# Performance work log

Measured on AMD Instinct MI355X. Metric: run time of the kernel, lower is better.

The kernel has to match this reference:

```python
import jax, jax.numpy as jnp
import numpy as np

NQ = 6; DM = 128; CH = 4; SEQ = 2048; CHUNK = 16; BATCH = 128
NFP = 5 * NQ * 2   # feature params for 2 layers
NMP = 5 * NQ * 2   # mixing params for 2 layers

# ---- batched gate matrices (theta: (B,)) ----

def _rx(t):
    c = jnp.cos(t / 2).astype(jnp.complex64)
    s = (-1j * jnp.sin(t / 2)).astype(jnp.complex64)
    return jnp.stack([jnp.stack([c, s], -1), jnp.stack([s, c], -1)], -2)

def _ry(t):
    c = jnp.cos(t / 2).astype(jnp.complex64)
    s = jnp.sin(t / 2).astype(jnp.complex64)
    return jnp.stack([jnp.stack([c, -s], -1), jnp.stack([s, c], -1)], -2)

def _rz(t):
    e = jnp.exp(-1j * t.astype(jnp.complex64) / 2)
    z = jnp.zeros_like(e)
    return jnp.stack([jnp.stack([e, z], -1), jnp.stack([z, jnp.conj(e)], -1)], -2)

def _crx(t):
    B = t.shape[0]
    r = _rx(t)
    I = jnp.broadcast_to(jnp.eye(2, dtype=jnp.complex64), (B, 2, 2))
    Z = jnp.zeros((B, 2, 2), jnp.complex64)
    return jnp.concatenate([jnp.concatenate([I, Z], -1), jnp.concatenate([Z, r], -1)], -2)

# ---- batched statevector gate application; state: (B, 2, ..., 2) with axis 1+w = wire w ----

def _ap1(s, U, w):
    s = jnp.moveaxis(s, 1 + w, 1)
    sh = s.shape
    s = jnp.einsum('bij,bjr->bir', U, s.reshape(sh[0], 2, -1)).reshape(sh)
    return jnp.moveaxis(s, 1, 1 + w)

def _ap2(s, U, w0, w1):
    s = jnp.moveaxis(s, (1 + w0, 1 + w1), (1, 2))
    sh = s.shape
    s = jnp.einsum('bij,bjr->bir', U, s.reshape(sh[0], 4, -1)).reshape(sh)
    return jnp.moveaxis(s, (1, 2), (1 + w0, 1 + w1))

def _ansatz(s, p, off):
    # RX,RY,RZ on each qubit, then forward CRX ring, then backward CRX ring
    for i in range(NQ):
        s = _ap1(s, _rx(p[:, off + 3 * i]), i)
        s = _ap1(s, _ry(p[:, off + 3 * i + 1]), i)
        s = _ap1(s, _rz(p[:, off + 3 * i + 2]), i)
    off += 3 * NQ
    for i in range(NQ):
        s = _ap2(s, _crx(p[:, off]), i, (i + 1) % NQ)
        off += 1
    for i in range(NQ - 1, -1, -1):
        s = _ap2(s, _crx(p[:, off]), i, (i - 1) % NQ)
        off += 1
    return s, off

def _circuit(angles, fp, mp):
    B = angles.shape[0]
    s = jnp.zeros((B, 2 ** NQ), jnp.complex64).at[:, 0].set(1.0).reshape((B,) + (2,) * NQ)
    for i in range(NQ):                      # RY input embedding
        s = _ap1(s, _ry(angles[:, i]), i)
    off = 0
    for _ in range(2):                        # feature layers
        s, off = _ansatz(s, fp, off)
    off = 0
    for _ in range(2):                        # mixing layers
        s, off = _ansatz(s, mp, off)
    xs, ys, zs = [], [], []
    for i in range(NQ):                       # <X_i>, <Y_i>, <Z_i>
        v = jnp.moveaxis(s, 1 + i, 1).reshape(B, 2, -1)
        a, b = v[:, 0], v[:, 1]
        ab = jnp.sum(jnp.conj(a) * b, -1)
        xs.append(2 * jnp.real(ab))
        ys.append(2 * jnp.imag(ab))
        zs.append(jnp.sum(jnp.abs(a) ** 2 - jnp.abs(b) ** 2, -1))
    return jnp.stack(xs + ys + zs, 1)         # (B, 18) ordered X..Y..Z

def _ln(x, g, b, eps=1e-5):
    m = x.mean(-1, keepdims=True)
    v = ((x - m) ** 2).mean(-1, keepdims=True)
    return (x - m) / jnp.sqrt(v + eps) * g + b

def _fwd(x, conv_w, conv_b, ln1_g, ln1_b, ca1_w, ca1_b, ca2_w, ca2_b, pp_w, pp_b,
         ep_w, ep_b, op_w, op_b, ln2_g, ln2_b, sa1_w, sa1_b, sa2_w, sa2_b,
         cl1_w, cl1_b, cl2_w, cl2_b):
    B, C, S = x.shape
    h = jax.lax.conv_general_dilated(x, conv_w, (1,), [(1, 1)],
                                     dimension_numbers=('NCH', 'OIH', 'NCH')) + conv_b[None, :, None]
    h = jnp.transpose(h, (0, 2, 1))           # (B, S, D)
    h = _ln(h, ln1_g, ln1_b)
    nchunks = S // CHUNK
    h = h.reshape(B * nchunks, CHUNK, DM)
    sc = jnp.tanh(h @ ca1_w + ca1_b) @ ca2_w + ca2_b
    w = jax.nn.softmax(sc, axis=1)
    summ = jnp.sum(w * h, axis=1)             # (B*nchunks, D)
    ap = summ @ pp_w + pp_b
    fp, mp = ap[:, :NFP], ap[:, NFP:]
    ang = jnp.tanh(summ @ ep_w + ep_b) * np.pi
    q = _circuit(ang, fp, mp)                 # (B*nchunks, 18)
    cf = jax.nn.silu(_ln(q @ op_w + op_b, ln2_g, ln2_b))  # dropout = eval identity
    cf = cf.reshape(B, nchunks, DM)
    ss = jnp.tanh(cf @ sa1_w + sa1_b) @ sa2_w + sa2_b
    sw = jax.nn.softmax(ss, axis=1)
    rep = jnp.sum(sw * cf, axis=1)
    return jax.nn.silu(rep @ cl1_w + cl1_b) @ cl2_w + cl2_b

def setup_inputs() -> dict:
    key = jax.random.key(0)
    ks = jax.random.split(key, 16)
    n = lambda k, sh: (jax.random.normal(k, sh, jnp.float32) * 0.05)
    return {
        'x': jax.random.normal(ks[0], (BATCH, CH, SEQ), jnp.float32),
        'conv_w': n(ks[1], (DM, CH, 3)), 'conv_b': jnp.zeros((DM,), jnp.float32),
        'ln1_g': jnp.ones((DM,), jnp.float32), 'ln1_b': jnp.zeros((DM,), jnp.float32),
        'ca1_w': n(ks[2], (DM, DM // 4)), 'ca1_b': jnp.zeros((DM // 4,), jnp.float32),
        'ca2_w': n(ks[3], (DM // 4, 1)), 'ca2_b': jnp.zeros((1,), jnp.float32),
        'pp_w': n(ks[4], (DM, NFP + NMP)), 'pp_b': jnp.zeros((NFP + NMP,), jnp.float32),
        'ep_w': n(ks[5], (DM, NQ)), 'ep_b': jnp.zeros((NQ,), jnp.float32),
        'op_w': n(ks[6], (3 * NQ, DM)), 'op_b': jnp.zeros((DM,), jnp.float32),
        'ln2_g': jnp.ones((DM,), jnp.float32), 'ln2_b': jnp.zeros((DM,), jnp.float32),
        'sa1_w': n(ks[7], (DM, DM // 4)), 'sa1_b': jnp.zeros((DM // 4,), jnp.float32),
        'sa2_w': n(ks[8], (DM // 4, 1)), 'sa2_b': jnp.zeros((1,), jnp.float32),
        'cl1_w': n(ks[9], (DM, DM // 2)), 'cl1_b': jnp.zeros((DM // 2,), jnp.float32),
        'cl2_w': n(ks[10], (DM // 2, 2)), 'cl2_b': jnp.zeros((2,), jnp.float32),
    }

def reference(x, conv_w, conv_b, ln1_g, ln1_b, ca1_w, ca1_b, ca2_w, ca2_b, pp_w, pp_b,
              ep_w, ep_b, op_w, op_b, ln2_g, ln2_b, sa1_w, sa1_b, sa2_w, sa2_b,
              cl1_w, cl1_b, cl2_w, cl2_b):
    return _fwd(x, conv_w, conv_b, ln1_g, ln1_b, ca1_w, ca1_b, ca2_w, ca2_b, pp_w, pp_b,
                ep_w, ep_b, op_w, op_b, ln2_g, ln2_b, sa1_w, sa1_b, sa2_w, sa2_b,
                cl1_w, cl1_b, cl2_w, cl2_b)
```

## Files before the change

### kernel.cpp

```cpp
#include <hip/hip_runtime.h>
#include <math.h>


constexpr int kNQ    = 6;
constexpr int kDM    = 128;
constexpr int kCH    = 4;
constexpr int kSEQ   = 2048;
constexpr int kCHUNK = 16;
constexpr int kBATCH = 128;
constexpr int kNCH   = kSEQ / kCHUNK;
constexpr int kNP    = 120;
constexpr float kPI  = 3.14159265358979323846f;

typedef __attribute__((ext_vector_type(8))) short bf16x8;
typedef __attribute__((ext_vector_type(4))) float f32x4;

__device__ __forceinline__ float fast_tanh(float x) {
  float e = __expf(-2.f * fabsf(x));
  float r = (1.f - e) * __builtin_amdgcn_rcpf(1.f + e);
  return copysignf(r, x);
}
__device__ __forceinline__ float fast_silu(float x) {
  return x * __builtin_amdgcn_rcpf(1.f + __expf(-x));
}

template <int XM>
__device__ __forceinline__ float qp(float v) {
  constexpr int ctrl = (XM == 1) ? 0xB1 : 0x4E;
  return __int_as_float(
      __builtin_amdgcn_update_dpp(0, __float_as_int(v), ctrl, 0xF, 0xF, true));
}


template <int RB>
__device__ __forceinline__ void rx_reg(float c, float s, float* sr, float* si) {
#pragma unroll
  for (int r0 = 0; r0 < 16; ++r0) {
    if (r0 & RB) continue;
    int r1 = r0 | RB;
    float ar = sr[r0], ai = si[r0], br = sr[r1], bi = si[r1];
    sr[r0] = fmaf(c, ar,  s * bi);  si[r0] = fmaf(c, ai, -s * br);
    sr[r1] = fmaf(c, br,  s * ai);  si[r1] = fmaf(c, bi, -s * ar);
  }
}

template <int RB>
__device__ __forceinline__ void ry_reg(float c, float s, float* sr, float* si) {
#pragma unroll
  for (int r0 = 0; r0 < 16; ++r0) {
    if (r0 & RB) continue;
    int r1 = r0 | RB;
    float ar = sr[r0], ai = si[r0], br = sr[r1], bi = si[r1];
    sr[r0] = fmaf(c, ar, -s * br);  si[r0] = fmaf(c, ai, -s * bi);
    sr[r1] = fmaf(s, ar,  c * br);  si[r1] = fmaf(s, ai,  c * bi);
  }
}

template <int RB>
__device__ __forceinline__ void rz_reg(float c, float s, float* sr, float* si) {
#pragma unroll
  for (int r = 0; r < 16; ++r) {
    float sp = (r & RB) ? s : -s;
    float ar = sr[r], ai = si[r];
    sr[r] = fmaf(c, ar, -sp * ai);
    si[r] = fmaf(c, ai,  sp * ar);
  }
}

template <int XM>
__device__ __forceinline__ void rx_lane(float c, float s, float* sr, float* si) {
#pragma unroll
  for (int r = 0; r < 16; ++r) {
    float pr = qp<XM>(sr[r]), pi = qp<XM>(si[r]);
    sr[r] = fmaf(c, sr[r],  s * pi);
    si[r] = fmaf(c, si[r], -s * pr);
  }
}

template <int XM>
__device__ __forceinline__ void ry_lane(float c, float sg, float* sr, float* si) {
#pragma unroll
  for (int r = 0; r < 16; ++r) {
    float pr = qp<XM>(sr[r]), pi = qp<XM>(si[r]);
    sr[r] = fmaf(c, sr[r], sg * pr);
    si[r] = fmaf(c, si[r], sg * pi);
  }
}

__device__ __forceinline__ void rz_lane(float c, float sp, float* sr, float* si) {
#pragma unroll
  for (int r = 0; r < 16; ++r) {
    float ar = sr[r], ai = si[r];
    sr[r] = fmaf(c, ar, -sp * ai);
    si[r] = fmaf(c, ai,  sp * ar);
  }
}

template <int RB, int CB>
__device__ __forceinline__ void crx_reg_reg(float c, float s, float* sr, float* si) {
#pragma unroll
  for (int r0 = 0; r0 < 16; ++r0) {
    if ((r0 & RB) || !(r0 & CB)) continue;
    int r1 = r0 | RB;
    float ar = sr[r0], ai = si[r0], br = sr[r1], bi = si[r1];
    sr[r0] = fmaf(c, ar,  s * bi);  si[r0] = fmaf(c, ai, -s * br);
    sr[r1] = fmaf(c, br,  s * ai);  si[r1] = fmaf(c, bi, -s * ar);
  }
}

template <int XM, int CB>
__device__ __forceinline__ void crx_reg_lane(float c, float s, float* sr, float* si) {
#pragma unroll
  for (int r = 0; r < 16; ++r) {
    if (!(r & CB)) continue;
    float pr = qp<XM>(sr[r]), pi = qp<XM>(si[r]);
    sr[r] = fmaf(c, sr[r],  s * pi);
    si[r] = fmaf(c, si[r], -s * pr);
  }
}

template <int RB>
__device__ __forceinline__ void meas_reg(const float* sr, const float* si,
                                         float& tr, float& ti, float& zz) {
  tr = 0.f; ti = 0.f; zz = 0.f;
#pragma unroll
  for (int r0 = 0; r0 < 16; ++r0) {
    float n = fmaf(sr[r0], sr[r0], si[r0] * si[r0]);
    zz += (r0 & RB) ? -n : n;
    if (r0 & RB) continue;
    int r1 = r0 | RB;
    tr = fmaf(sr[r0], sr[r1], fmaf(si[r0], si[r1], tr));
    ti = fmaf(sr[r0], si[r1], fmaf(-si[r0], sr[r1], ti));
  }
  tr += qp<1>(tr); tr += qp<2>(tr);
  ti += qp<1>(ti); ti += qp<2>(ti);
  zz += qp<1>(zz); zz += qp<2>(zz);
}


__global__ __launch_bounds__(128) void k_pre8(
    const float* __restrict__ x,
    const float* __restrict__ conv_w, const float* __restrict__ conv_b,
    const float* __restrict__ ln1_g,  const float* __restrict__ ln1_b,
    const float* __restrict__ ca1_w,  const float* __restrict__ ca1_b,
    const float* __restrict__ ca2_w,  const float* __restrict__ ca2_b,
    const float* __restrict__ pp_w,   const float* __restrict__ pp_b,
    const float* __restrict__ ep_w,   const float* __restrict__ ep_b,
    float* __restrict__ outb, int emit_cs)
{
  constexpr int NC = 8;

  __shared__ __align__(16) float xs[kCH][NC * kCHUNK + 4];
  __shared__ __align__(16) float hbuf[kCHUNK][132];
  __shared__ __align__(16) float spart[2][16];
  __shared__ __align__(16) float wl[kCHUNK];
  __shared__ __align__(16) float sums[NC][kDM];
  __shared__ float mrow[kCHUNK], irow[kCHUNK];

  const int tid    = threadIdx.x;
  const int chunk0 = blockIdx.x * NC;
  const int b      = chunk0 >> 7;
  const int tloc   = (chunk0 & 127) * kCHUNK;
  const int d      = tid;
  const int lane   = tid & 63;
  const int wv     = tid >> 6;
  const int col    = (lane & 15) + 16 * wv;
  const int qd     = lane >> 4;

  float w12[12];
  {
    const float4* cw = (const float4*)(conv_w + d * 12);
    float4 a0 = cw[0], a1 = cw[1], a2 = cw[2];
    w12[0]=a0.x; w12[1]=a0.y; w12[2]=a0.z; w12[3]=a0.w;
    w12[4]=a1.x; w12[5]=a1.y; w12[6]=a1.z; w12[7]=a1.w;
    w12[8]=a2.x; w12[9]=a2.y; w12[10]=a2.z; w12[11]=a2.w;
  }
  float cb = conv_b[d];
  float g1 = ln1_g[d], b1 = ln1_b[d];
  float cb1 = ca1_b[col], cw2 = ca2_w[col], cb2 = ca2_b[0];

  bf16x8 bhi[4], blo[4];
#pragma unroll
  for (int ks = 0; ks < 4; ++ks)
#pragma unroll
    for (int jj = 0; jj < 8; ++jj) {
      float bvf = ca1_w[(ks * 32 + qd * 8 + jj) * 32 + col];
      unsigned bb = __float_as_uint(bvf);
      bhi[ks][jj] = (short)(bb >> 16);
      float lf = bvf - __uint_as_float(bb & 0xffff0000u);
      blo[ks][jj] = (short)(__float_as_uint(lf) >> 16);
    }

#pragma unroll
  for (int ch = 0; ch < kCH; ++ch) {
#pragma unroll
    for (int base = 0; base < 2; ++base) {
      int pos = base * 128 + tid;
      if (pos < NC * kCHUNK + 2) {
        int s = tloc - 1 + pos;
        float v = 0.f;
        if (s >= 0 && s < kSEQ) v = x[((size_t)b * kCH + ch) * kSEQ + s];
        xs[ch][pos] = v;
      }
    }
  }
  __syncthreads();

  for (int c = 0; c < NC; ++c) {
    float h[kCHUNK];
#pragma unroll
    for (int t = 0; t < kCHUNK; ++t) h[t] = cb;
#pragma unroll
    for (int ch = 0; ch < kCH; ++ch) {
      const float4* xp = (const float4*)&xs[ch][c * kCHUNK];
      float4 v0 = xp[0], v1 = xp[1], v2 = xp[2], v3 = xp[3], v4 = xp[4];
      float xr[18];
      xr[0]=v0.x; xr[1]=v0.y; xr[2]=v0.z; xr[3]=v0.w;
      xr[4]=v1.x; xr[5]=v1.y; xr[6]=v1.z; xr[7]=v1.w;
      xr[8]=v2.x; xr[9]=v2.y; xr[10]=v2.z; xr[11]=v2.w;
      xr[12]=v3.x; xr[13]=v3.y; xr[14]=v3.z; xr[15]=v3.w;
      xr[16]=v4.x; xr[17]=v4.y;
      float c0 = w12[ch*3+0], c1 = w12[ch*3+1], c2 = w12[ch*3+2];
#pragma unroll
      for (int t = 0; t < kCHUNK; ++t)
        h[t] = fmaf(xr[t], c0, fmaf(xr[t+1], c1, fmaf(xr[t+2], c2, h[t])));
    }
#pragma unroll
    for (int t = 0; t < kCHUNK; ++t) hbuf[t][d] = h[t];
    __syncthreads();

    {
      int row = tid >> 3, k = tid & 7;
      const float4* rp = (const float4*)&hbuf[row][k * 16];
      float s1 = 0.f, s2 = 0.f;
#pragma unroll
      for (int q = 0; q < 4; ++q) {
        float4 v = rp[q];
        s1 += v.x + v.y + v.z + v.w;
        s2 = fmaf(v.x,v.x,s2); s2 = fmaf(v.y,v.y,s2);
        s2 = fmaf(v.z,v.z,s2); s2 = fmaf(v.w,v.w,s2);
      }
#pragma unroll
      for (int o = 1; o < 8; o <<= 1) {
        s1 += __shfl_xor(s1, o, 64);
        s2 += __shfl_xor(s2, o, 64);
      }
      if (k == 0) {
        float m = s1 * (1.f / kDM);
        mrow[row] = m;
        irow[row] = rsqrtf(s2 * (1.f / kDM) - m * m + 1e-5f);
      }
    }
    __syncthreads();

#pragma unroll
    for (int t = 0; t < kCHUNK; ++t) {
      h[t] = fmaf((h[t] - mrow[t]) * irow[t], g1, b1);
      unsigned hb = __float_as_uint(h[t]);
      float lof = h[t] - __uint_as_float(hb & 0xffff0000u);
      unsigned pk = (hb >> 16) | (__float_as_uint(lof) & 0xffff0000u);
      ((unsigned*)&hbuf[t][0])[d] = pk;
    }
    __syncthreads();

    f32x4 acc = {0.f, 0.f, 0.f, 0.f};
    {
      const unsigned* hrow = (const unsigned*)&hbuf[lane & 15][0];
#pragma unroll
      for (int ks = 0; ks < 4; ++ks) {
        const uint4* ap = (const uint4*)(hrow + ks * 32 + qd * 8);
        uint4 w0 = ap[0], w1 = ap[1];
        bf16x8 ahi, alo;
        ahi[0] = (short)(w0.x & 0xffff); ahi[1] = (short)(w0.y & 0xffff);
        ahi[2] = (short)(w0.z & 0xffff); ahi[3] = (short)(w0.w & 0xffff);
        ahi[4] = (short)(w1.x & 0xffff); ahi[5] = (short)(w1.y & 0xffff);
        ahi[6] = (short)(w1.z & 0xffff); ahi[7] = (short)(w1.w & 0xffff);
        alo[0] = (short)(w0.x >> 16); alo[1] = (short)(w0.y >> 16);
        alo[2] = (short)(w0.z >> 16); alo[3] = (short)(w0.w >> 16);
        alo[4] = (short)(w1.x >> 16); alo[5] = (short)(w1.y >> 16);
        alo[6] = (short)(w1.z >> 16); alo[7] = (short)(w1.w >> 16);
        acc = __builtin_amdgcn_mfma_f32_16x16x32_bf16(ahi, bhi[ks], acc, 0, 0, 0);
        acc = __builtin_amdgcn_mfma_f32_16x16x32_bf16(ahi, blo[ks], acc, 0, 0, 0);
        acc = __builtin_amdgcn_mfma_f32_16x16x32_bf16(alo, bhi[ks], acc, 0, 0, 0);
      }
    }

    {
      float ev[4];
#pragma unroll
      for (int r = 0; r < 4; ++r)
        ev[r] = fast_tanh(acc[r] + cb1) * cw2;
#pragma unroll
      for (int o = 1; o < 16; o <<= 1)
#pragma unroll
        for (int r = 0; r < 4; ++r) ev[r] += __shfl_xor(ev[r], o, 64);
      if ((lane & 15) == 0)
        *(float4*)&spart[wv][qd * 4] = make_float4(ev[0], ev[1], ev[2], ev[3]);
    }
    __syncthreads();

    if (tid < 16) {
      float scl = spart[0][tid] + spart[1][tid] + cb2;
      float mx = scl;
#pragma unroll
      for (int o = 1; o < 16; o <<= 1) mx = fmaxf(mx, __shfl_xor(mx, o, 64));
      float e = __expf(scl - mx);
      float se = e;
#pragma unroll
      for (int o = 1; o < 16; o <<= 1) se += __shfl_xor(se, o, 64);
      wl[tid] = e * (1.f / se);
    }
    __syncthreads();

    {
      const float4* w4 = (const float4*)wl;
      float4 wa = w4[0], wb = w4[1], wc = w4[2], wd = w4[3];
      float acc2 = 0.f;
      acc2 = fmaf(wa.x, h[0],  acc2); acc2 = fmaf(wa.y, h[1],  acc2);
      acc2 = fmaf(wa.z, h[2],  acc2); acc2 = fmaf(wa.w, h[3],  acc2);
      acc2 = fmaf(wb.x, h[4],  acc2); acc2 = fmaf(wb.y, h[5],  acc2);
      acc2 = fmaf(wb.z, h[6],  acc2); acc2 = fmaf(wb.w, h[7],  acc2);
      acc2 = fmaf(wc.x, h[8],  acc2); acc2 = fmaf(wc.y, h[9],  acc2);
      acc2 = fmaf(wc.z, h[10], acc2); acc2 = fmaf(wc.w, h[11], acc2);
      acc2 = fmaf(wd.x, h[12], acc2); acc2 = fmaf(wd.y, h[13], acc2);
      acc2 = fmaf(wd.z, h[14], acc2); acc2 = fmaf(wd.w, h[15], acc2);
      sums[c][d] = acc2;
    }
  }
  __syncthreads();

  if (tid < kNP + kNQ) {
    const bool isep = (tid >= kNP);
    const int  jj   = tid - kNP;
    const float* wp = isep ? (ep_w + jj) : (pp_w + tid);
    const int  ws   = isep ? kNQ : kNP;
    const int  ws2  = ws * 2, ws3 = ws * 3, ws4 = ws * 4;
    float bias = isep ? ep_b[jj] : pp_b[tid];
    float accp[NC];
#pragma unroll
    for (int c = 0; c < NC; ++c) accp[c] = bias;
#pragma unroll 4
    for (int q4 = 0; q4 < 32; ++q4) {
      float w0 = wp[0], w1 = wp[ws], w2 = wp[ws2], w3 = wp[ws3];
      wp += ws4;
#pragma unroll
      for (int c = 0; c < NC; ++c) {
        float4 s = *(const float4*)&sums[c][q4 * 4];
        accp[c] = fmaf(s.x, w0, fmaf(s.y, w1, fmaf(s.z, w2, fmaf(s.w, w3, accp[c]))));
      }
    }
    const int slot = isep ? jj : (6 + tid);
#pragma unroll
    for (int c = 0; c < NC; ++c) {
      int chunkg = chunk0 + c;
      float ha = isep ? (0.5f * fast_tanh(accp[c]) * kPI) : (0.5f * accp[c]);
      if (emit_cs) {
        ((float2*)(outb + (size_t)chunkg * 256))[slot] =
            make_float2(__cosf(ha), __sinf(ha));
      } else {
        outb[(size_t)chunkg * 126 + slot] = ha;
      }
    }
  }
}


constexpr int kCsStride = 260;

__global__ __launch_bounds__(64) void k_circ_cs(const float* __restrict__ csA,
                                                float* __restrict__ qv_g)
{
  __shared__ __align__(16) float lds[16 * kCsStride];

  const int lane  = threadIdx.x;
  const int c     = lane >> 2;
  const int l     = lane & 3;
  const int chunk = blockIdx.x * 16 + c;
  const int b0 = (l >> 1) & 1;
  const int b1 = l & 1;

  {
    const float4* src = (const float4*)(csA + (size_t)blockIdx.x * 16 * 256);
#pragma unroll
    for (int i = 0; i < 16; ++i) {
      float4 v = src[i * 64 + lane];
      *(float4*)&lds[i * kCsStride + lane * 4] = v;
    }
  }
  __syncthreads();

  const float2* cp = (const float2*)&lds[c * kCsStride];

  float sr[16], si[16];
#pragma unroll
  for (int r = 0; r < 16; ++r) { sr[r] = 0.f; si[r] = 0.f; }
  sr[0] = (l == 0) ? 1.f : 0.f;

  {
    float2 q0 = cp[0], q1 = cp[1], q2 = cp[2], q3 = cp[3], q4 = cp[4], q5 = cp[5];
    ry_lane<2>(q0.x, b0 ? q0.y : -q0.y, sr, si);
    ry_lane<1>(q1.x, b1 ? q1.y : -q1.y, sr, si);
    ry_reg<8>(q2.x, q2.y, sr, si);
    ry_reg<4>(q3.x, q3.y, sr, si);
    ry_reg<2>(q4.x, q4.y, sr, si);
    ry_reg<1>(q5.x, q5.y, sr, si);
  }

  for (int a = 0; a < 4; ++a) {
    const float2* pb = cp + 6 + a * 30;
    float2 t;
    t = pb[0];  rx_lane<2>(t.x, t.y, sr, si);
    t = pb[1];  ry_lane<2>(t.x, b0 ? t.y : -t.y, sr, si);
    t = pb[2];  rz_lane   (t.x, b0 ? t.y : -t.y, sr, si);
    t = pb[3];  rx_lane<1>(t.x, t.y, sr, si);
    t = pb[4];  ry_lane<1>(t.x, b1 ? t.y : -t.y, sr, si);
    t = pb[5];  rz_lane   (t.x, b1 ? t.y : -t.y, sr, si);
    t = pb[6];  rx_reg<8>(t.x, t.y, sr, si);
    t = pb[7];  ry_reg<8>(t.x, t.y, sr, si);
    t = pb[8];  rz_reg<8>(t.x, t.y, sr, si);
    t = pb[9];  rx_reg<4>(t.x, t.y, sr, si);
    t = pb[10]; ry_reg<4>(t.x, t.y, sr, si);
    t = pb[11]; rz_reg<4>(t.x, t.y, sr, si);
    t = pb[12]; rx_reg<2>(t.x, t.y, sr, si);
    t = pb[13]; ry_reg<2>(t.x, t.y, sr, si);
    t = pb[14]; rz_reg<2>(t.x, t.y, sr, si);
    t = pb[15]; rx_reg<1>(t.x, t.y, sr, si);
    t = pb[16]; ry_reg<1>(t.x, t.y, sr, si);
    t = pb[17]; rz_reg<1>(t.x, t.y, sr, si);
    t = pb[18]; { float c2 = b0 ? t.x : 1.f, s2 = b0 ? t.y : 0.f; rx_lane<1>(c2, s2, sr, si); }
    t = pb[19]; { float c2 = b1 ? t.x : 1.f, s2 = b1 ? t.y : 0.f; rx_reg<8>(c2, s2, sr, si); }
    t = pb[20]; crx_reg_reg<4, 8>(t.x, t.y, sr, si);
    t = pb[21]; crx_reg_reg<2, 4>(t.x, t.y, sr, si);
    t = pb[22]; crx_reg_reg<1, 2>(t.x, t.y, sr, si);
    t = pb[23]; crx_reg_lane<2, 1>(t.x, t.y, sr, si);
    t = pb[24]; crx_reg_reg<2, 1>(t.x, t.y, sr, si);
    t = pb[25]; crx_reg_reg<4, 2>(t.x, t.y, sr, si);
    t = pb[26]; crx_reg_reg<8, 4>(t.x, t.y, sr, si);
    t = pb[27]; crx_reg_lane<1, 8>(t.x, t.y, sr, si);
    t = pb[28]; { float c2 = b1 ? t.x : 1.f, s2 = b1 ? t.y : 0.f; rx_lane<2>(c2, s2, sr, si); }
    t = pb[29]; { float c2 = b0 ? t.x : 1.f, s2 = b0 ? t.y : 0.f; rx_reg<1>(c2, s2, sr, si); }
  }

  float res[18];
  {
    float tr = 0.f, ti = 0.f, zz = 0.f;
#pragma unroll
    for (int r = 0; r < 16; ++r) {
      float pr = qp<2>(sr[r]), pi = qp<2>(si[r]);
      tr = fmaf(sr[r], pr, fmaf(si[r], pi, tr));
      ti = fmaf(sr[r], pi, fmaf(-si[r], pr, ti));
      zz = fmaf(sr[r], sr[r], fmaf(si[r], si[r], zz));
    }
    tr = b0 ? 0.f : tr;  ti = b0 ? 0.f : ti;  zz = b0 ? -zz : zz;
    tr += qp<1>(tr); tr += qp<2>(tr);
    ti += qp<1>(ti); ti += qp<2>(ti);
    zz += qp<1>(zz); zz += qp<2>(zz);
    res[0] = 2.f * tr; res[6] = 2.f * ti; res[12] = zz;
  }
  {
    float tr = 0.f, ti = 0.f, zz = 0.f;
#pragma unroll
    for (int r = 0; r < 16; ++r) {
      float pr = qp<1>(sr[r]), pi = qp<1>(si[r]);
      tr = fmaf(sr[r], pr, fmaf(si[r], pi, tr));
      ti = fmaf(sr[r], pi, fmaf(-si[r], pr, ti));
      zz = fmaf(sr[r], sr[r], fmaf(si[r], si[r], zz));
    }
    tr = b1 ? 0.f : tr;  ti = b1 ? 0.f : ti;  zz = b1 ? -zz : zz;
    tr += qp<1>(tr); tr += qp<2>(tr);
    ti += qp<1>(ti); ti += qp<2>(ti);
    zz += qp<1>(zz); zz += qp<2>(zz);
    res[1] = 2.f * tr; res[7] = 2.f * ti; res[13] = zz;
  }
  {
    float tr, ti, zz;
    meas_reg<8>(sr, si, tr, ti, zz); res[2] = 2.f*tr; res[8]  = 2.f*ti; res[14] = zz;
    meas_reg<4>(sr, si, tr, ti, zz); res[3] = 2.f*tr; res[9]  = 2.f*ti; res[15] = zz;
    meas_reg<2>(sr, si, tr, ti, zz); res[4] = 2.f*tr; res[10] = 2.f*ti; res[16] = zz;
    meas_reg<1>(sr, si, tr, ti, zz); res[5] = 2.f*tr; res[11] = 2.f*ti; res[17] = zz;
  }
  if (l == 0) {
    float* qo = qv_g + (size_t)chunk * 18;
#pragma unroll
    for (int k = 0; k < 18; ++k) qo[k] = res[k];
  }
}


__global__ __launch_bounds__(64) void k_circ(const float* __restrict__ csb_g,
                                             float* __restrict__ qv_g)
{
  const int lane  = threadIdx.x;
  const int c     = lane >> 2;
  const int l     = lane & 3;
  const int chunk = blockIdx.x * 16 + c;
  const float* cp = csb_g + (size_t)chunk * 126;
  const int b0 = (l >> 1) & 1;
  const int b1 = l & 1;

  float sr[16], si[16];
#pragma unroll
  for (int r = 0; r < 16; ++r) { sr[r] = 0.f; si[r] = 0.f; }
  sr[0] = (l == 0) ? 1.f : 0.f;

  {
    float gc[6], gs[6];
#pragma unroll
    for (int g = 0; g < 6; ++g) { float th = cp[g]; gc[g] = __cosf(th); gs[g] = __sinf(th); }
    ry_lane<2>(gc[0], b0 ? gs[0] : -gs[0], sr, si);
    ry_lane<1>(gc[1], b1 ? gs[1] : -gs[1], sr, si);
    ry_reg<8>(gc[2], gs[2], sr, si);
    ry_reg<4>(gc[3], gs[3], sr, si);
    ry_reg<2>(gc[4], gs[4], sr, si);
    ry_reg<1>(gc[5], gs[5], sr, si);
  }

  for (int a = 0; a < 4; ++a) {
    const float* pb = cp + 6 + a * 30;
    float gc[30], gs[30];
#pragma unroll
    for (int g = 0; g < 30; ++g) { float th = pb[g]; gc[g] = __cosf(th); gs[g] = __sinf(th); }
    rx_lane<2>(gc[0], gs[0], sr, si);
    ry_lane<2>(gc[1], b0 ? gs[1] : -gs[1], sr, si);
    rz_lane   (gc[2], b0 ? gs[2] : -gs[2], sr, si);
    rx_lane<1>(gc[3], gs[3], sr, si);
    ry_lane<1>(gc[4], b1 ? gs[4] : -gs[4], sr, si);
    rz_lane   (gc[5], b1 ? gs[5] : -gs[5], sr, si);
    rx_reg<8>(gc[6],  gs[6],  sr, si);  ry_reg<8>(gc[7],  gs[7],  sr, si);  rz_reg<8>(gc[8],  gs[8],  sr, si);
    rx_reg<4>(gc[9],  gs[9],  sr, si);  ry_reg<4>(gc[10], gs[10], sr, si);  rz_reg<4>(gc[11], gs[11], sr, si);
    rx_reg<2>(gc[12], gs[12], sr, si);  ry_reg<2>(gc[13], gs[13], sr, si);  rz_reg<2>(gc[14], gs[14], sr, si);
    rx_reg<1>(gc[15], gs[15], sr, si);  ry_reg<1>(gc[16], gs[16], sr, si);  rz_reg<1>(gc[17], gs[17], sr, si);
    { float c2 = b0 ? gc[18] : 1.f, s2 = b0 ? gs[18] : 0.f; rx_lane<1>(c2, s2, sr, si); }
    { float c2 = b1 ? gc[19] : 1.f, s2 = b1 ? gs[19] : 0.f; rx_reg<8>(c2, s2, sr, si); }
    crx_reg_reg<4, 8>(gc[20], gs[20], sr, si);
    crx_reg_reg<2, 4>(gc[21], gs[21], sr, si);
    crx_reg_reg<1, 2>(gc[22], gs[22], sr, si);
    crx_reg_lane<2, 1>(gc[23], gs[23], sr, si);
    crx_reg_reg<2, 1>(gc[24], gs[24], sr, si);
    crx_reg_reg<4, 2>(gc[25], gs[25], sr, si);
    crx_reg_reg<8, 4>(gc[26], gs[26], sr, si);
    crx_reg_lane<1, 8>(gc[27], gs[27], sr, si);
    { float c2 = b1 ? gc[28] : 1.f, s2 = b1 ? gs[28] : 0.f; rx_lane<2>(c2, s2, sr, si); }
    { float c2 = b0 ? gc[29] : 1.f, s2 = b0 ? gs[29] : 0.f; rx_reg<1>(c2, s2, sr, si); }
  }

  float res[18];
  {
    float tr = 0.f, ti = 0.f, zz = 0.f;
#pragma unroll
    for (int r = 0; r < 16; ++r) {
      float pr = qp<2>(sr[r]), pi = qp<2>(si[r]);
      tr = fmaf(sr[r], pr, fmaf(si[r], pi, tr));
      ti = fmaf(sr[r], pi, fmaf(-si[r], pr, ti));
      zz = fmaf(sr[r], sr[r], fmaf(si[r], si[r], zz));
    }
    tr = b0 ? 0.f : tr;  ti = b0 ? 0.f : ti;  zz = b0 ? -zz : zz;
    tr += qp<1>(tr); tr += qp<2>(tr);
    ti += qp<1>(ti); ti += qp<2>(ti);
    zz += qp<1>(zz); zz += qp<2>(zz);
    res[0] = 2.f * tr; res[6] = 2.f * ti; res[12] = zz;
  }
  {
    float tr = 0.f, ti = 0.f, zz = 0.f;
#pragma unroll
    for (int r = 0; r < 16; ++r) {
      float pr = qp<1>(sr[r]), pi = qp<1>(si[r]);
      tr = fmaf(sr[r], pr, fmaf(si[r], pi, tr));
      ti = fmaf(sr[r], pi, fmaf(-si[r], pr, ti));
      zz = fmaf(sr[r], sr[r], fmaf(si[r], si[r], zz));
    }
    tr = b1 ? 0.f : tr;  ti = b1 ? 0.f : ti;  zz = b1 ? -zz : zz;
    tr += qp<1>(tr); tr += qp<2>(tr);
    ti += qp<1>(ti); ti += qp<2>(ti);
    zz += qp<1>(zz); zz += qp<2>(zz);
    res[1] = 2.f * tr; res[7] = 2.f * ti; res[13] = zz;
  }
  {
    float tr, ti, zz;
    meas_reg<8>(sr, si, tr, ti, zz); res[2] = 2.f*tr; res[8]  = 2.f*ti; res[14] = zz;
    meas_reg<4>(sr, si, tr, ti, zz); res[3] = 2.f*tr; res[9]  = 2.f*ti; res[15] = zz;
    meas_reg<2>(sr, si, tr, ti, zz); res[4] = 2.f*tr; res[10] = 2.f*ti; res[16] = zz;
    meas_reg<1>(sr, si, tr, ti, zz); res[5] = 2.f*tr; res[11] = 2.f*ti; res[17] = zz;
  }
  if (l == 0) {
    float* qo = qv_g + (size_t)chunk * 18;
#pragma unroll
    for (int k = 0; k < 18; ++k) qo[k] = res[k];
  }
}


__global__ __launch_bounds__(128) void k_post(
    const float* __restrict__ qv_g,
    const float* __restrict__ op_w, const float* __restrict__ op_b,
    const float* __restrict__ ln2_g, const float* __restrict__ ln2_b,
    const float* __restrict__ sa1_w, const float* __restrict__ sa1_b,
    const float* __restrict__ sa2_w, const float* __restrict__ sa2_b,
    float* __restrict__ cf, float* __restrict__ sclb)
{
  __shared__ float cfs[132];
  __shared__ float part1[32];
  __shared__ float red[4];

  const int chunk = blockIdx.x, tid = threadIdx.x, d = tid;
  const int j = tid & 31, sub = tid >> 5;

  float qv[18];
  {
    const float* qpp = qv_g + (size_t)chunk * 18;
#pragma unroll
    for (int k = 0; k < 18; ++k) qv[k] = qpp[k];
  }
  float acc = op_b[d];
#pragma unroll
  for (int k = 0; k < 18; ++k) acc = fmaf(qv[k], op_w[k * kDM + d], acc);

  float v = acc, v2 = acc * acc;
#pragma unroll
  for (int o = 32; o; o >>= 1) { v += __shfl_xor(v, o, 64); v2 += __shfl_xor(v2, o, 64); }
  if ((tid & 63) == 0) { red[tid >> 6] = v; red[2 + (tid >> 6)] = v2; }
  __syncthreads();
  float s1 = red[0] + red[1], s2 = red[2] + red[3];
  float m = s1 * (1.f / kDM);
  float var = s2 * (1.f / kDM) - m * m;
  float xn = fmaf((acc - m) * rsqrtf(var + 1e-5f), ln2_g[d], ln2_b[d]);
  float cfv = fast_silu(xn);
  cf[(size_t)chunk * kDM + d] = cfv;
  cfs[d] = cfv;
  __syncthreads();

  float acc2 = 0.f;
  {
    const float* wp2 = sa1_w + (sub * 32) * 32 + j;
#pragma unroll
    for (int q = 0; q < 8; ++q) {
      float4 hv = *(const float4*)&cfs[sub * 32 + q * 4];
      acc2 = fmaf(hv.x, wp2[(q*4+0)*32], acc2);
      acc2 = fmaf(hv.y, wp2[(q*4+1)*32], acc2);
      acc2 = fmaf(hv.z, wp2[(q*4+2)*32], acc2);
      acc2 = fmaf(hv.w, wp2[(q*4+3)*32], acc2);
    }
  }
  acc2 += __shfl_xor(acc2, 32, 64);
  if (sub == 2) part1[j] = acc2;
  __syncthreads();
  if (tid < 32) {
    float hv = fast_tanh(acc2 + part1[j] + sa1_b[j]) * sa2_w[j];
#pragma unroll
    for (int o = 16; o; o >>= 1) hv += __shfl_xor(hv, o, 64);
    if (j == 0) sclb[chunk] = hv + sa2_b[0];
  }
}


__global__ __launch_bounds__(512) void k_pool_cf(
    const float* __restrict__ cf, const float* __restrict__ scl,
    const float* __restrict__ cl1_w, const float* __restrict__ cl1_b,
    const float* __restrict__ cl2_w, const float* __restrict__ cl2_b,
    float* __restrict__ out)
{
  __shared__ float wl[kNCH];
  __shared__ float rep4[4][kDM];
  __shared__ float ulp[8][64];
  __shared__ float ul[64];
  __shared__ float red2[16];
  int b = blockIdx.x, tid = threadIdx.x;
  int idx = tid & 127, wid = tid >> 6;
  float s = scl[b*kNCH + idx];
  float mx = s;
#pragma unroll
  for (int o = 32; o; o >>= 1) mx = fmaxf(mx, __shfl_xor(mx,o,64));
  if ((tid & 63) == 0) red2[wid] = mx;
  __syncthreads();
  mx = fmaxf(red2[0], red2[1]);
  float e = __expf(s - mx);
  float se = e;
#pragma unroll
  for (int o = 32; o; o >>= 1) se += __shfl_xor(se,o,64);
  if ((tid & 63) == 0) red2[8+wid] = se;
  if (tid < kNCH) wl[tid] = e;
  __syncthreads();
  float inv = 1.f/(red2[8]+red2[9]);
  {
    int dd = tid & 127, qq = tid >> 7;
    const float* cfb = cf + (size_t)b*kNCH*kDM + (size_t)qq*32*kDM;
    const float* wlq = wl + qq*32;
    float a0=0,a1=0,a2=0,a3=0;
#pragma unroll 4
    for (int ncc = 0; ncc < 32; ncc += 4) {
      a0 = fmaf(wlq[ncc+0], cfb[(ncc+0)*kDM+dd], a0);
      a1 = fmaf(wlq[ncc+1], cfb[(ncc+1)*kDM+dd], a1);
      a2 = fmaf(wlq[ncc+2], cfb[(ncc+2)*kDM+dd], a2);
      a3 = fmaf(wlq[ncc+3], cfb[(ncc+3)*kDM+dd], a3);
    }
    rep4[qq][dd] = (a0+a1)+(a2+a3);
  }
  __syncthreads();
  {
    int jj = tid & 63, qq = tid >> 6;
    float accp = 0.f;
#pragma unroll
    for (int k = 0; k < 16; ++k) {
      int dd = qq*16 + k;
      float rv = ((rep4[0][dd]+rep4[1][dd])+(rep4[2][dd]+rep4[3][dd]))*inv;
      accp = fmaf(rv, cl1_w[dd*64+jj], accp);
    }
    ulp[qq][jj] = accp;
  }
  __syncthreads();
  if (tid < 64) {
    float acc = cl1_b[tid];
#pragma unroll
    for (int q = 0; q < 8; ++q) acc += ulp[q][tid];
    ul[tid] = fast_silu(acc);
  }
  __syncthreads();
  if (tid < 2) {
    float acc = cl2_b[tid];
#pragma unroll
    for (int k = 0; k < 64; ++k) acc = fmaf(ul[k], cl2_w[k*2+tid], acc);
    out[b*2+tid] = acc;
  }
}


__device__ __forceinline__ void fb_rx(float2 cs, int w, int lane, float& ar, float& ai) {
  int m = 1 << (5 - w);
  float pr = __shfl_xor(ar, m, 64), pi = __shfl_xor(ai, m, 64);
  float nr = fmaf(cs.x, ar, cs.y * pi), ni = fmaf(cs.x, ai, -cs.y * pr);
  ar = nr; ai = ni;
}
__device__ __forceinline__ void fb_ry(float2 cs, int w, int lane, float& ar, float& ai) {
  int m = 1 << (5 - w);
  float pr = __shfl_xor(ar, m, 64), pi = __shfl_xor(ai, m, 64);
  float sg = ((lane >> (5 - w)) & 1) ? cs.y : -cs.y;
  float nr = fmaf(cs.x, ar, sg * pr), ni = fmaf(cs.x, ai, sg * pi);
  ar = nr; ai = ni;
}
__device__ __forceinline__ void fb_rz(float2 cs, int w, int lane, float& ar, float& ai) {
  float sp = ((lane >> (5 - w)) & 1) ? cs.y : -cs.y;
  float nr = fmaf(ar, cs.x, -ai * sp), ni = fmaf(ar, sp, ai * cs.x);
  ar = nr; ai = ni;
}
__device__ __forceinline__ void fb_crx(float2 cs, int w0, int w1, int lane, float& ar, float& ai) {
  int m = 1 << (5 - w1);
  float pr = __shfl_xor(ar, m, 64), pi = __shfl_xor(ai, m, 64);
  if ((lane >> (5 - w0)) & 1) {
    float nr = fmaf(cs.x, ar, cs.y * pi), ni = fmaf(cs.x, ai, -cs.y * pr);
    ar = nr; ai = ni;
  }
}
__device__ __forceinline__ void fb_ansatz(const float2* cs, int lane, float& ar, float& ai) {
#pragma unroll
  for (int i = 0; i < kNQ; ++i) {
    fb_rx(cs[3*i+0], i, lane, ar, ai);
    fb_ry(cs[3*i+1], i, lane, ar, ai);
    fb_rz(cs[3*i+2], i, lane, ar, ai);
  }
  int off = 18;
#pragma unroll
  for (int i = 0; i < kNQ; ++i) fb_crx(cs[off++], i, (i+1)%kNQ, lane, ar, ai);
#pragma unroll
  for (int i = kNQ-1; i >= 0; --i) fb_crx(cs[off++], i, (i+5)%kNQ, lane, ar, ai);
}

__global__ __launch_bounds__(128) void k_chunk_fb(
    const float* __restrict__ x,
    const float* __restrict__ conv_w, const float* __restrict__ conv_b,
    const float* __restrict__ ln1_g,  const float* __restrict__ ln1_b,
    const float* __restrict__ ca1_w,  const float* __restrict__ ca1_b,
    const float* __restrict__ ca2_w,  const float* __restrict__ ca2_b,
    const float* __restrict__ pp_w,   const float* __restrict__ pp_b,
    const float* __restrict__ ep_w,   const float* __restrict__ ep_b,
    const float* __restrict__ op_w,   const float* __restrict__ op_b,
    const float* __restrict__ ln2_g,  const float* __restrict__ ln2_b,
    float* __restrict__ cf)
{
  __shared__ float hbuf[kCHUNK][132];
  __shared__ __align__(16) float Bu[512];
  __shared__ float mrow[kCHUNK], irow[kCHUNK];
  __shared__ float red[4];
  float (*xs)[kCHUNK+2] = (float(*)[kCHUNK+2])Bu;
  float (*part)[32] = (float(*)[32])Bu;
  float* summ = Bu; float* wl = Bu + 128; float* qv = Bu + 144;
  float2* csb = (float2*)(Bu + 164);

  const int tid = threadIdx.x, chunk = blockIdx.x;
  const int b = chunk >> 7, nc = chunk & 127, t0 = nc * kCHUNK, d = tid;
  const int j = tid & 31, sub = tid >> 5;

  float w12[12];
  {
    const float4* cw = (const float4*)(conv_w + d*12);
    float4 a0=cw[0],a1=cw[1],a2=cw[2];
    w12[0]=a0.x;w12[1]=a0.y;w12[2]=a0.z;w12[3]=a0.w;
    w12[4]=a1.x;w12[5]=a1.y;w12[6]=a1.z;w12[7]=a1.w;
    w12[8]=a2.x;w12[9]=a2.y;w12[10]=a2.z;w12[11]=a2.w;
  }
  float cb = conv_b[d], g1 = ln1_g[d], b1 = ln1_b[d];
  float wreg[32];
  { const float* wp = ca1_w + (sub*32)*32 + j;
#pragma unroll
    for (int k = 0; k < 32; ++k) wreg[k] = wp[k*32]; }

  if (tid < kCH*(kCHUNK+2)) {
    int ch = tid/(kCHUNK+2), pos = tid%(kCHUNK+2), s = t0-1+pos;
    float v = 0.f; if (s >= 0 && s < kSEQ) v = x[(b*kCH+ch)*kSEQ + s];
    xs[ch][pos] = v;
  }
  __syncthreads();
#pragma unroll
  for (int t = 0; t < kCHUNK; ++t) {
    float acc = cb;
#pragma unroll
    for (int ch = 0; ch < kCH; ++ch)
#pragma unroll
      for (int k = 0; k < 3; ++k) acc = fmaf(xs[ch][t+k], w12[ch*3+k], acc);
    hbuf[t][d] = acc;
  }
  __syncthreads();
  {
    int row = tid >> 3, k = tid & 7;
    const float4* rp = (const float4*)&hbuf[row][k*16];
    float s1 = 0.f, s2 = 0.f;
#pragma unroll
    for (int q = 0; q < 4; ++q) {
      float4 v = rp[q];
      s1 += v.x+v.y+v.z+v.w;
      s2 = fmaf(v.x,v.x,s2); s2 = fmaf(v.y,v.y,s2);
      s2 = fmaf(v.z,v.z,s2); s2 = fmaf(v.w,v.w,s2);
    }
#pragma unroll
    for (int o = 1; o < 8; o <<= 1) { s1 += __shfl_xor(s1,o,64); s2 += __shfl_xor(s2,o,64); }
    if (k == 0) {
      float m = s1*(1.f/kDM);
      mrow[row] = m; irow[row] = rsqrtf(s2*(1.f/kDM) - m*m + 1e-5f);
    }
  }
  __syncthreads();
#pragma unroll
  for (int t = 0; t < kCHUNK; ++t)
    hbuf[t][d] = fmaf((hbuf[t][d]-mrow[t])*irow[t], g1, b1);
  __syncthreads();
  float p[kCHUNK];
#pragma unroll
  for (int t = 0; t < kCHUNK; ++t) {
    float acc = 0.f;
#pragma unroll
    for (int qq = 0; qq < 8; ++qq) {
      int q = (qq + 2*sub) & 7;
      float4 v = *(const float4*)&hbuf[t][sub*32 + q*4];
      acc = fmaf(v.x,wreg[q*4+0],acc); acc = fmaf(v.y,wreg[q*4+1],acc);
      acc = fmaf(v.z,wreg[q*4+2],acc); acc = fmaf(v.w,wreg[q*4+3],acc);
    }
    p[t] = acc;
  }
#pragma unroll
  for (int t = 0; t < kCHUNK; ++t) p[t] += __shfl_xor(p[t], 32, 64);
  if (sub == 2) {
#pragma unroll
    for (int t = 0; t < kCHUNK; ++t) part[t][j] = p[t];
  }
  __syncthreads();
  if (tid < 64) {
    float bj = ca1_b[j], w2 = ca2_w[j];
#pragma unroll
    for (int t = 0; t < kCHUNK; ++t) p[t] = fast_tanh(p[t] + part[t][j] + bj) * w2;
#pragma unroll
    for (int o = 16; o; o >>= 1)
#pragma unroll
      for (int t = 0; t < kCHUNK; ++t) p[t] += __shfl_xor(p[t], o, 64);
    float mx = p[0];
#pragma unroll
    for (int t = 1; t < kCHUNK; ++t) mx = fmaxf(mx, p[t]);
    float e[kCHUNK], ssum = 0.f;
#pragma unroll
    for (int t = 0; t < kCHUNK; ++t) { e[t] = __expf(p[t]-mx); ssum += e[t]; }
    float inv = 1.f/ssum;
    if (tid == 0) {
      float4* w4 = (float4*)wl;
      w4[0]=make_float4(e[0]*inv,e[1]*inv,e[2]*inv,e[3]*inv);
      w4[1]=make_float4(e[4]*inv,e[5]*inv,e[6]*inv,e[7]*inv);
      w4[2]=make_float4(e[8]*inv,e[9]*inv,e[10]*inv,e[11]*inv);
      w4[3]=make_float4(e[12]*inv,e[13]*inv,e[14]*inv,e[15]*inv);
    }
  }
  __syncthreads();
  {
    float acc = 0.f;
    const float4* w4 = (const float4*)wl;
#pragma unroll
    for (int tq = 0; tq < 4; ++tq) {
      float4 wv = w4[tq];
      acc = fmaf(wv.x,hbuf[tq*4+0][d],acc); acc = fmaf(wv.y,hbuf[tq*4+1][d],acc);
      acc = fmaf(wv.z,hbuf[tq*4+2][d],acc); acc = fmaf(wv.w,hbuf[tq*4+3][d],acc);
    }
    summ[d] = acc;
  }
  __syncthreads();
  if (tid < kNP) {
    float acc = pp_b[tid];
    const float4* s4 = (const float4*)summ;
#pragma unroll 8
    for (int q = 0; q < 32; ++q) {
      float4 v = s4[q];
      acc = fmaf(v.x,pp_w[(q*4+0)*kNP+tid],acc); acc = fmaf(v.y,pp_w[(q*4+1)*kNP+tid],acc);
      acc = fmaf(v.z,pp_w[(q*4+2)*kNP+tid],acc); acc = fmaf(v.w,pp_w[(q*4+3)*kNP+tid],acc);
    }
    csb[6+tid] = make_float2(__cosf(0.5f*acc), __sinf(0.5f*acc));
  } else if (tid < kNP + kNQ) {
    int jj = tid - kNP;
    float acc = ep_b[jj];
    for (int dd = 0; dd < kDM; ++dd) acc = fmaf(summ[dd], ep_w[dd*kNQ+jj], acc);
    float a = fast_tanh(acc) * kPI;
    csb[jj] = make_float2(__cosf(0.5f*a), __sinf(0.5f*a));
  }
  float ow[18];
#pragma unroll
  for (int jj = 0; jj < 18; ++jj) ow[jj] = op_w[jj*kDM + d];
  float g2 = ln2_g[d], b2 = ln2_b[d], ob = op_b[d];
  __syncthreads();
  if (tid < 64) {
    int lane = tid;
    float ar = (lane == 0) ? 1.f : 0.f, ai = 0.f;
#pragma unroll
    for (int i = 0; i < kNQ; ++i) fb_ry(csb[i], i, lane, ar, ai);
    fb_ansatz(csb+6, lane, ar, ai);  fb_ansatz(csb+36, lane, ar, ai);
    fb_ansatz(csb+66, lane, ar, ai); fb_ansatz(csb+96, lane, ar, ai);
#pragma unroll
    for (int i = 0; i < kNQ; ++i) {
      int m = 1 << (5-i);
      float pr = __shfl_xor(ar, m, 64), pi = __shfl_xor(ai, m, 64);
      int bit = (lane >> (5-i)) & 1;
      float nrm = fmaf(ar,ar,ai*ai);
      float abr, abi, zz;
      if (bit) { abr = 0.f; abi = 0.f; zz = -nrm; }
      else { abr = fmaf(ar,pr,ai*pi); abi = fmaf(ar,pi,-ai*pr); zz = nrm; }
#pragma unroll
      for (int o = 32; o; o >>= 1) {
        abr += __shfl_xor(abr,o,64); abi += __shfl_xor(abi,o,64); zz += __shfl_xor(zz,o,64);
      }
      if (lane == 0) { qv[i] = 2.f*abr; qv[kNQ+i] = 2.f*abi; qv[2*kNQ+i] = zz; }
    }
  }
  __syncthreads();
  {
    float acc = ob;
#pragma unroll
    for (int jj = 0; jj < 18; ++jj) acc = fmaf(qv[jj], ow[jj], acc);
    float v = acc, v2 = acc*acc;
#pragma unroll
    for (int o = 32; o; o >>= 1) { v += __shfl_xor(v,o,64); v2 += __shfl_xor(v2,o,64); }
    if ((tid & 63) == 0) { red[tid>>6] = v; red[2+(tid>>6)] = v2; }
    __syncthreads();
    float s1 = red[0]+red[1], s2 = red[2]+red[3];
    float m = s1*(1.f/kDM), var = s2*(1.f/kDM) - m*m;
    float xn = fmaf((acc-m)*rsqrtf(var+1e-5f), g2, b2);
    cf[(size_t)chunk*kDM + d] = fast_silu(xn);
  }
}

__global__ __launch_bounds__(256) void k_scl_fb(
    const float* __restrict__ cf,
    const float* __restrict__ sa1_w, const float* __restrict__ sa1_b,
    const float* __restrict__ sa2_w, const float* __restrict__ sa2_b,
    float* __restrict__ scl)
{
  int tid = threadIdx.x, wid = tid >> 6, lane = tid & 63;
  int pair = blockIdx.x * 4 + wid;
  int j = lane & 31, hh = lane >> 5;
  const float4* row = (const float4*)(cf + (size_t)pair*kDM + hh*64);
  const float* wp = sa1_w + (hh*64)*32 + j;
  float acc = 0.f;
#pragma unroll
  for (int q = 0; q < 16; ++q) {
    float4 v = row[q];
    acc = fmaf(v.x,wp[(q*4+0)*32],acc); acc = fmaf(v.y,wp[(q*4+1)*32],acc);
    acc = fmaf(v.z,wp[(q*4+2)*32],acc); acc = fmaf(v.w,wp[(q*4+3)*32],acc);
  }
  acc += __shfl_xor(acc, 32, 64);
  float hv = fast_tanh(acc + sa1_b[j]);
  float v = hv * sa2_w[j];
#pragma unroll
  for (int o = 16; o; o >>= 1) v += __shfl_xor(v, o, 64);
  if (lane == 0) scl[pair] = v + sa2_b[0];
}


extern "C" void kernel_launch(void* const* d_in, const int* in_sizes, int n_in,
                              void* d_out, int out_size, void* d_ws, size_t ws_size,
                              hipStream_t stream) {
  const float* x      = (const float*)d_in[0];
  const float* conv_w = (const float*)d_in[1];
  const float* conv_b = (const float*)d_in[2];
  const float* ln1_g  = (const float*)d_in[3];
  const float* ln1_b  = (const float*)d_in[4];
  const float* ca1_w  = (const float*)d_in[5];
  const float* ca1_b  = (const float*)d_in[6];
  const float* ca2_w  = (const float*)d_in[7];
  const float* ca2_b  = (const float*)d_in[8];
  const float* pp_w   = (const float*)d_in[9];
  const float* pp_b   = (const float*)d_in[10];
  const float* ep_w   = (const float*)d_in[11];
  const float* ep_b   = (const float*)d_in[12];
  const float* op_w   = (const float*)d_in[13];
  const float* op_b   = (const float*)d_in[14];
  const float* ln2_g  = (const float*)d_in[15];
  const float* ln2_b  = (const float*)d_in[16];
  const float* sa1_w  = (const float*)d_in[17];
  const float* sa1_b  = (const float*)d_in[18];
  const float* sa2_w  = (const float*)d_in[19];
  const float* sa2_b  = (const float*)d_in[20];
  const float* cl1_w  = (const float*)d_in[21];
  const float* cl1_b  = (const float*)d_in[22];
  const float* cl2_w  = (const float*)d_in[23];
  const float* cl2_b  = (const float*)d_in[24];
  float* out = (float*)d_out;

  const size_t nch   = (size_t)kBATCH * kNCH;
  const size_t fCS   = nch * 256;
  const size_t need1 = (fCS + nch * 18 + nch) * sizeof(float);
  const size_t fA    = nch * kDM;
  const size_t need2 = (fA + nch * 18 + nch) * sizeof(float);

  if (ws_size >= need1) {
    float* csA   = (float*)d_ws;
    float* cf    = csA;
    float* qv_g  = csA + fCS;
    float* sclb  = qv_g + nch * 18;
    k_pre8<<<(kBATCH * kNCH) / 8, 128, 0, stream>>>(
        x, conv_w, conv_b, ln1_g, ln1_b, ca1_w, ca1_b, ca2_w, ca2_b,
        pp_w, pp_b, ep_w, ep_b, csA, 1);
    k_circ_cs<<<(kBATCH * kNCH) / 16, 64, 0, stream>>>(csA, qv_g);
    k_post<<<kBATCH * kNCH, 128, 0, stream>>>(
        qv_g, op_w, op_b, ln2_g, ln2_b, sa1_w, sa1_b, sa2_w, sa2_b, cf, sclb);
    k_pool_cf<<<kBATCH, 512, 0, stream>>>(
        cf, sclb, cl1_w, cl1_b, cl2_w, cl2_b, out);
  } else if (ws_size >= need2) {
    float* A     = (float*)d_ws;
    float* qv_g  = A + fA;
    float* sclb  = qv_g + nch * 18;
    k_pre8<<<(kBATCH * kNCH) / 8, 128, 0, stream>>>(
        x, conv_w, conv_b, ln1_g, ln1_b, ca1_w, ca1_b, ca2_w, ca2_b,
        pp_w, pp_b, ep_w, ep_b, A, 0);
    k_circ<<<(kBATCH * kNCH) / 16, 64, 0, stream>>>(A, qv_g);
    k_post<<<kBATCH * kNCH, 128, 0, stream>>>(
        qv_g, op_w, op_b, ln2_g, ln2_b, sa1_w, sa1_b, sa2_w, sa2_b, A, sclb);
    k_pool_cf<<<kBATCH, 512, 0, stream>>>(
        A, sclb, cl1_w, cl1_b, cl2_w, cl2_b, out);
  } else {
    float* cf   = (float*)d_ws;
    float* sclb = cf + nch * kDM;
    k_chunk_fb<<<kBATCH * kNCH, 128, 0, stream>>>(
        x, conv_w, conv_b, ln1_g, ln1_b, ca1_w, ca1_b, ca2_w, ca2_b,
        pp_w, pp_b, ep_w, ep_b, op_w, op_b, ln2_g, ln2_b, cf);
    k_scl_fb<<<(kBATCH * kNCH) / 4, 256, 0, stream>>>(cf, sa1_w, sa1_b, sa2_w, sa2_b, sclb);
    k_pool_cf<<<kBATCH, 512, 0, stream>>>(cf, sclb, cl1_w, cl1_b, cl2_w, cl2_b, out);
  }
}
```

Measured before the change: 208.2 us.

## Fuse pre, circuit and post kernels into one megakernel per 16 chunks

Merges the conv/LN/attention-pool/param-projection kernel, the statevector circuit simulation and the post-projection/score kernel into a single kernel handling 16 chunks per block. Circuit inputs (cos/sin) and measured expectations stay in shared memory instead of round-tripping through global workspace, and three launches become one. The circuit phase now runs only on 64 of 128 threads, and the post phase loops serially over 16 chunks with barriers. That cuts parallelism and grid size (1024 blocks) and may lower occupancy because of the larger LDS footprint.

Result: slower. 213.8 us (+2.7%).

```diff
diff --git a/kernel.cpp b/kernel.cpp
--- a/kernel.cpp
+++ b/kernel.cpp
@@ -138,259 +138,9 @@
 }
 
 
-__global__ __launch_bounds__(128) void k_pre8(
-    const float* __restrict__ x,
-    const float* __restrict__ conv_w, const float* __restrict__ conv_b,
-    const float* __restrict__ ln1_g,  const float* __restrict__ ln1_b,
-    const float* __restrict__ ca1_w,  const float* __restrict__ ca1_b,
-    const float* __restrict__ ca2_w,  const float* __restrict__ ca2_b,
-    const float* __restrict__ pp_w,   const float* __restrict__ pp_b,
-    const float* __restrict__ ep_w,   const float* __restrict__ ep_b,
-    float* __restrict__ outb, int emit_cs)
-{
-  constexpr int NC = 8;
-
-  __shared__ __align__(16) float xs[kCH][NC * kCHUNK + 4];
-  __shared__ __align__(16) float hbuf[kCHUNK][132];
-  __shared__ __align__(16) float spart[2][16];
-  __shared__ __align__(16) float wl[kCHUNK];
-  __shared__ __align__(16) float sums[NC][kDM];
-  __shared__ float mrow[kCHUNK], irow[kCHUNK];
-
-  const int tid    = threadIdx.x;
-  const int chunk0 = blockIdx.x * NC;
-  const int b      = chunk0 >> 7;
-  const int tloc   = (chunk0 & 127) * kCHUNK;
-  const int d      = tid;
-  const int lane   = tid & 63;
-  const int wv     = tid >> 6;
-  const int col    = (lane & 15) + 16 * wv;
-  const int qd     = lane >> 4;
-
-  float w12[12];
-  {
-    const float4* cw = (const float4*)(conv_w + d * 12);
-    float4 a0 = cw[0], a1 = cw[1], a2 = cw[2];
-    w12[0]=a0.x; w12[1]=a0.y; w12[2]=a0.z; w12[3]=a0.w;
-    w12[4]=a1.x; w12[5]=a1.y; w12[6]=a1.z; w12[7]=a1.w;
-    w12[8]=a2.x; w12[9]=a2.y; w12[10]=a2.z; w12[11]=a2.w;
-  }
-  float cb = conv_b[d];
-  float g1 = ln1_g[d], b1 = ln1_b[d];
-  float cb1 = ca1_b[col], cw2 = ca2_w[col], cb2 = ca2_b[0];
-
-  bf16x8 bhi[4], blo[4];
-#pragma unroll
-  for (int ks = 0; ks < 4; ++ks)
-#pragma unroll
-    for (int jj = 0; jj < 8; ++jj) {
-      float bvf = ca1_w[(ks * 32 + qd * 8 + jj) * 32 + col];
-      unsigned bb = __float_as_uint(bvf);
-      bhi[ks][jj] = (short)(bb >> 16);
-      float lf = bvf - __uint_as_float(bb & 0xffff0000u);
-      blo[ks][jj] = (short)(__float_as_uint(lf) >> 16);
-    }
-
-#pragma unroll
-  for (int ch = 0; ch < kCH; ++ch) {
-#pragma unroll
-    for (int base = 0; base < 2; ++base) {
-      int pos = base * 128 + tid;
-      if (pos < NC * kCHUNK + 2) {
-        int s = tloc - 1 + pos;
-        float v = 0.f;
-        if (s >= 0 && s < kSEQ) v = x[((size_t)b * kCH + ch) * kSEQ + s];
-        xs[ch][pos] = v;
-      }
-    }
-  }
-  __syncthreads();
-
-  for (int c = 0; c < NC; ++c) {
-    float h[kCHUNK];
-#pragma unroll
-    for (int t = 0; t < kCHUNK; ++t) h[t] = cb;
-#pragma unroll
-    for (int ch = 0; ch < kCH; ++ch) {
-      const float4* xp = (const float4*)&xs[ch][c * kCHUNK];
-      float4 v0 = xp[0], v1 = xp[1], v2 = xp[2], v3 = xp[3], v4 = xp[4];
-      float xr[18];
-      xr[0]=v0.x; xr[1]=v0.y; xr[2]=v0.z; xr[3]=v0.w;
-      xr[4]=v1.x; xr[5]=v1.y; xr[6]=v1.z; xr[7]=v1.w;
-      xr[8]=v2.x; xr[9]=v2.y; xr[10]=v2.z; xr[11]=v2.w;
-      xr[12]=v3.x; xr[13]=v3.y; xr[14]=v3.z; xr[15]=v3.w;
-      xr[16]=v4.x; xr[17]=v4.y;
-      float c0 = w12[ch*3+0], c1 = w12[ch*3+1], c2 = w12[ch*3+2];
-#pragma unroll
-      for (int t = 0; t < kCHUNK; ++t)
-        h[t] = fmaf(xr[t], c0, fmaf(xr[t+1], c1, fmaf(xr[t+2], c2, h[t])));
-    }
-#pragma unroll
-    for (int t = 0; t < kCHUNK; ++t) hbuf[t][d] = h[t];
-    __syncthreads();
-
-    {
-      int row = tid >> 3, k = tid & 7;
-      const float4* rp = (const float4*)&hbuf[row][k * 16];
-      float s1 = 0.f, s2 = 0.f;
-#pragma unroll
-      for (int q = 0; q < 4; ++q) {
-        float4 v = rp[q];
-        s1 += v.x + v.y + v.z + v.w;
-        s2 = fmaf(v.x,v.x,s2); s2 = fmaf(v.y,v.y,s2);
-        s2 = fmaf(v.z,v.z,s2); s2 = fmaf(v.w,v.w,s2);
-      }
-#pragma unroll
-      for (int o = 1; o < 8; o <<= 1) {
-        s1 += __shfl_xor(s1, o, 64);
-        s2 += __shfl_xor(s2, o, 64);
-      }
-      if (k == 0) {
-        float m = s1 * (1.f / kDM);
-        mrow[row] = m;
-        irow[row] = rsqrtf(s2 * (1.f / kDM) - m * m + 1e-5f);
-      }
-    }
-    __syncthreads();
-
-#pragma unroll
-    for (int t = 0; t < kCHUNK; ++t) {
-      h[t] = fmaf((h[t] - mrow[t]) * irow[t], g1, b1);
-      unsigned hb = __float_as_uint(h[t]);
-      float lof = h[t] - __uint_as_float(hb & 0xffff0000u);
-      unsigned pk = (hb >> 16) | (__float_as_uint(lof) & 0xffff0000u);
-      ((unsigned*)&hbuf[t][0])[d] = pk;
-    }
-    __syncthreads();
-
-    f32x4 acc = {0.f, 0.f, 0.f, 0.f};
-    {
-      const unsigned* hrow = (const unsigned*)&hbuf[lane & 15][0];
-#pragma unroll
-      for (int ks = 0; ks < 4; ++ks) {
-        const uint4* ap = (const uint4*)(hrow + ks * 32 + qd * 8);
-        uint4 w0 = ap[0], w1 = ap[1];
-        bf16x8 ahi, alo;
-        ahi[0] = (short)(w0.x & 0xffff); ahi[1] = (short)(w0.y & 0xffff);
-        ahi[2] = (short)(w0.z & 0xffff); ahi[3] = (short)(w0.w & 0xffff);
-        ahi[4] = (short)(w1.x & 0xffff); ahi[5] = (short)(w1.y & 0xffff);
-        ahi[6] = (short)(w1.z & 0xffff); ahi[7] = (short)(w1.w & 0xffff);
-        alo[0] = (short)(w0.x >> 16); alo[1] = (short)(w0.y >> 16);
-        alo[2] = (short)(w0.z >> 16); alo[3] = (short)(w0.w >> 16);
-        alo[4] = (short)(w1.x >> 16); alo[5] = (short)(w1.y >> 16);
-        alo[6] = (short)(w1.z >> 16); alo[7] = (short)(w1.w >> 16);
-        acc = __builtin_amdgcn_mfma_f32_16x16x32_bf16(ahi, bhi[ks], acc, 0, 0, 0);
-        acc = __builtin_amdgcn_mfma_f32_16x16x32_bf16(ahi, blo[ks], acc, 0, 0, 0);
-        acc = __builtin_amdgcn_mfma_f32_16x16x32_bf16(alo, bhi[ks], acc, 0, 0, 0);
-      }
-    }
-
-    {
-      float ev[4];
-#pragma unroll
-      for (int r = 0; r < 4; ++r)
-        ev[r] = fast_tanh(acc[r] + cb1) * cw2;
-#pragma unroll
-      for (int o = 1; o < 16; o <<= 1)
-#pragma unroll
-        for (int r = 0; r < 4; ++r) ev[r] += __shfl_xor(ev[r], o, 64);
-      if ((lane & 15) == 0)
-        *(float4*)&spart[wv][qd * 4] = make_float4(ev[0], ev[1], ev[2], ev[3]);
-    }
-    __syncthreads();
-
-    if (tid < 16) {
-      float scl = spart[0][tid] + spart[1][tid] + cb2;
-      float mx = scl;
-#pragma unroll
-      for (int o = 1; o < 16; o <<= 1) mx = fmaxf(mx, __shfl_xor(mx, o, 64));
-      float e = __expf(scl - mx);
-      float se = e;
-#pragma unroll
-      for (int o = 1; o < 16; o <<= 1) se += __shfl_xor(se, o, 64);
-      wl[tid] = e * (1.f / se);
-    }
-    __syncthreads();
-
-    {
-      const float4* w4 = (const float4*)wl;
-      float4 wa = w4[0], wb = w4[1], wc = w4[2], wd = w4[3];
-      float acc2 = 0.f;
-      acc2 = fmaf(wa.x, h[0],  acc2); acc2 = fmaf(wa.y, h[1],  acc2);
-      acc2 = fmaf(wa.z, h[2],  acc2); acc2 = fmaf(wa.w, h[3],  acc2);
-      acc2 = fmaf(wb.x, h[4],  acc2); acc2 = fmaf(wb.y, h[5],  acc2);
-      acc2 = fmaf(wb.z, h[6],  acc2); acc2 = fmaf(wb.w, h[7],  acc2);
-      acc2 = fmaf(wc.x, h[8],  acc2); acc2 = fmaf(wc.y, h[9],  acc2);
-      acc2 = fmaf(wc.z, h[10], acc2); acc2 = fmaf(wc.w, h[11], acc2);
-      acc2 = fmaf(wd.x, h[12], acc2); acc2 = fmaf(wd.y, h[13], acc2);
-      acc2 = fmaf(wd.z, h[14], acc2); acc2 = fmaf(wd.w, h[15], acc2);
-      sums[c][d] = acc2;
-    }
-  }
-  __syncthreads();
-
-  if (tid < kNP + kNQ) {
-    const bool isep = (tid >= kNP);
-    const int  jj   = tid - kNP;
-    const float* wp = isep ? (ep_w + jj) : (pp_w + tid);
-    const int  ws   = isep ? kNQ : kNP;
-    const int  ws2  = ws * 2, ws3 = ws * 3, ws4 = ws * 4;
-    float bias = isep ? ep_b[jj] : pp_b[tid];
-    float accp[NC];
-#pragma unroll
-    for (int c = 0; c < NC; ++c) accp[c] = bias;
-#pragma unroll 4
-    for (int q4 = 0; q4 < 32; ++q4) {
-      float w0 = wp[0], w1 = wp[ws], w2 = wp[ws2], w3 = wp[ws3];
-      wp += ws4;
-#pragma unroll
-      for (int c = 0; c < NC; ++c) {
-        float4 s = *(const float4*)&sums[c][q4 * 4];
-        accp[c] = fmaf(s.x, w0, fmaf(s.y, w1, fmaf(s.z, w2, fmaf(s.w, w3, accp[c]))));
-      }
-    }
-    const int slot = isep ? jj : (6 + tid);
-#pragma unroll
-    for (int c = 0; c < NC; ++c) {
-      int chunkg = chunk0 + c;
-      float ha = isep ? (0.5f * fast_tanh(accp[c]) * kPI) : (0.5f * accp[c]);
-      if (emit_cs) {
-        ((float2*)(outb + (size_t)chunkg * 256))[slot] =
-            make_float2(__cosf(ha), __sinf(ha));
-      } else {
-        outb[(size_t)chunkg * 126 + slot] = ha;
-      }
-    }
-  }
-}
-
-
-constexpr int kCsStride = 260;
-
-__global__ __launch_bounds__(64) void k_circ_cs(const float* __restrict__ csA,
-                                                float* __restrict__ qv_g)
-{
-  __shared__ __align__(16) float lds[16 * kCsStride];
-
-  const int lane  = threadIdx.x;
-  const int c     = lane >> 2;
-  const int l     = lane & 3;
-  const int chunk = blockIdx.x * 16 + c;
-  const int b0 = (l >> 1) & 1;
-  const int b1 = l & 1;
-
-  {
-    const float4* src = (const float4*)(csA + (size_t)blockIdx.x * 16 * 256);
-#pragma unroll
-    for (int i = 0; i < 16; ++i) {
-      float4 v = src[i * 64 + lane];
-      *(float4*)&lds[i * kCsStride + lane * 4] = v;
-    }
-  }
-  __syncthreads();
-
-  const float2* cp = (const float2*)&lds[c * kCsStride];
-
+__device__ __forceinline__ void circ_from_cs(const float2* __restrict__ cp,
+                                             int l, int b0, int b1,
+                                             float* __restrict__ res) {
   float sr[16], si[16];
 #pragma unroll
   for (int r = 0; r < 16; ++r) { sr[r] = 0.f; si[r] = 0.f; }
@@ -441,7 +191,6 @@
     t = pb[29]; { float c2 = b0 ? t.x : 1.f, s2 = b0 ? t.y : 0.f; rx_reg<1>(c2, s2, sr, si); }
   }
 
-  float res[18];
   {
     float tr = 0.f, ti = 0.f, zz = 0.f;
 #pragma unroll
@@ -479,176 +228,311 @@
     meas_reg<2>(sr, si, tr, ti, zz); res[4] = 2.f*tr; res[10] = 2.f*ti; res[16] = zz;
     meas_reg<1>(sr, si, tr, ti, zz); res[5] = 2.f*tr; res[11] = 2.f*ti; res[17] = zz;
   }
-  if (l == 0) {
-    float* qo = qv_g + (size_t)chunk * 18;
-#pragma unroll
-    for (int k = 0; k < 18; ++k) qo[k] = res[k];
-  }
-}
-
-
-__global__ __launch_bounds__(64) void k_circ(const float* __restrict__ csb_g,
-                                             float* __restrict__ qv_g)
-{
-  const int lane  = threadIdx.x;
-  const int c     = lane >> 2;
-  const int l     = lane & 3;
-  const int chunk = blockIdx.x * 16 + c;
-  const float* cp = csb_g + (size_t)chunk * 126;
-  const int b0 = (l >> 1) & 1;
-  const int b1 = l & 1;
-
-  float sr[16], si[16];
-#pragma unroll
-  for (int r = 0; r < 16; ++r) { sr[r] = 0.f; si[r] = 0.f; }
-  sr[0] = (l == 0) ? 1.f : 0.f;
-
-  {
-    float gc[6], gs[6];
-#pragma unroll
-    for (int g = 0; g < 6; ++g) { float th = cp[g]; gc[g] = __cosf(th); gs[g] = __sinf(th); }
-    ry_lane<2>(gc[0], b0 ? gs[0] : -gs[0], sr, si);
-    ry_lane<1>(gc[1], b1 ? gs[1] : -gs[1], sr, si);
-    ry_reg<8>(gc[2], gs[2], sr, si);
-    ry_reg<4>(gc[3], gs[3], sr, si);
-    ry_reg<2>(gc[4], gs[4], sr, si);
-    ry_reg<1>(gc[5], gs[5], sr, si);
-  }
-
-  for (int a = 0; a < 4; ++a) {
-    const float* pb = cp + 6 + a * 30;
-    float gc[30], gs[30];
-#pragma unroll
-    for (int g = 0; g < 30; ++g) { float th = pb[g]; gc[g] = __cosf(th); gs[g] = __sinf(th); }
-    rx_lane<2>(gc[0], gs[0], sr, si);
-    ry_lane<2>(gc[1], b0 ? gs[1] : -gs[1], sr, si);
-    rz_lane   (gc[2], b0 ? gs[2] : -gs[2], sr, si);
-    rx_lane<1>(gc[3], gs[3], sr, si);
-    ry_lane<1>(gc[4], b1 ? gs[4] : -gs[4], sr, si);
-    rz_lane   (gc[5], b1 ? gs[5] : -gs[5], sr, si);
-    rx_reg<8>(gc[6],  gs[6],  sr, si);  ry_reg<8>(gc[7],  gs[7],  sr, si);  rz_reg<8>(gc[8],  gs[8],  sr, si);
-    rx_reg<4>(gc[9],  gs[9],  sr, si);  ry_reg<4>(gc[10], gs[10], sr, si);  rz_reg<4>(gc[11], gs[11], sr, si);
-    rx_reg<2>(gc[12], gs[12], sr, si);  ry_reg<2>(gc[13], gs[13], sr, si);  rz_reg<2>(gc[14], gs[14], sr, si);
-    rx_reg<1>(gc[15], gs[15], sr, si);  ry_reg<1>(gc[16], gs[16], sr, si);  rz_reg<1>(gc[17], gs[17], sr, si);
-    { float c2 = b0 ? gc[18] : 1.f, s2 = b0 ? gs[18] : 0.f; rx_lane<1>(c2, s2, sr, si); }
-    { float c2 = b1 ? gc[19] : 1.f, s2 = b1 ? gs[19] : 0.f; rx_reg<8>(c2, s2, sr, si); }
-    crx_reg_reg<4, 8>(gc[20], gs[20], sr, si);
-    crx_reg_reg<2, 4>(gc[21], gs[21], sr, si);
-    crx_reg_reg<1, 2>(gc[22], gs[22], sr, si);
-    crx_reg_lane<2, 1>(gc[23], gs[23], sr, si);
-    crx_reg_reg<2, 1>(gc[24], gs[24], sr, si);
-    crx_reg_reg<4, 2>(gc[25], gs[25], sr, si);
-    crx_reg_reg<8, 4>(gc[26], gs[26], sr, si);
-    crx_reg_lane<1, 8>(gc[27], gs[27], sr, si);
-    { float c2 = b1 ? gc[28] : 1.f, s2 = b1 ? gs[28] : 0.f; rx_lane<2>(c2, s2, sr, si); }
-    { float c2 = b0 ? gc[29] : 1.f, s2 = b0 ? gs[29] : 0.f; rx_reg<1>(c2, s2, sr, si); }
-  }
-
-  float res[18];
-  {
-    float tr = 0.f, ti = 0.f, zz = 0.f;
-#pragma unroll
-    for (int r = 0; r < 16; ++r) {
-      float pr = qp<2>(sr[r]), pi = qp<2>(si[r]);
-      tr = fmaf(sr[r], pr, fmaf(si[r], pi, tr));
-      ti = fmaf(sr[r], pi, fmaf(-si[r], pr, ti));
-      zz = fmaf(sr[r], sr[r], fmaf(si[r], si[r], zz));
-    }
-    tr = b0 ? 0.f : tr;  ti = b0 ? 0.f : ti;  zz = b0 ? -zz : zz;
-    tr += qp<1>(tr); tr += qp<2>(tr);
-    ti += qp<1>(ti); ti += qp<2>(ti);
-    zz += qp<1>(zz); zz += qp<2>(zz);
-    res[0] = 2.f * tr; res[6] = 2.f * ti; res[12] = zz;
-  }
-  {
-    float tr = 0.f, ti = 0.f, zz = 0.f;
-#pragma unroll
-    for (int r = 0; r < 16; ++r) {
-      float pr = qp<1>(sr[r]), pi = qp<1>(si[r]);
-      tr = fmaf(sr[r], pr, fmaf(si[r], pi, tr));
-      ti = fmaf(sr[r], pi, fmaf(-si[r], pr, ti));
-      zz = fmaf(sr[r], sr[r], fmaf(si[r], si[r], zz));
-    }
-    tr = b1 ? 0.f : tr;  ti = b1 ? 0.f : ti;  zz = b1 ? -zz : zz;
-    tr += qp<1>(tr); tr += qp<2>(tr);
-    ti += qp<1>(ti); ti += qp<2>(ti);
-    zz += qp<1>(zz); zz += qp<2>(zz);
-    res[1] = 2.f * tr; res[7] = 2.f * ti; res[13] = zz;
-  }
-  {
-    float tr, ti, zz;
-    meas_reg<8>(sr, si, tr, ti, zz); res[2] = 2.f*tr; res[8]  = 2.f*ti; res[14] = zz;
-    meas_reg<4>(sr, si, tr, ti, zz); res[3] = 2.f*tr; res[9]  = 2.f*ti; res[15] = zz;
-    meas_reg<2>(sr, si, tr, ti, zz); res[4] = 2.f*tr; res[10] = 2.f*ti; res[16] = zz;
-    meas_reg<1>(sr, si, tr, ti, zz); res[5] = 2.f*tr; res[11] = 2.f*ti; res[17] = zz;
-  }
-  if (l == 0) {
-    float* qo = qv_g + (size_t)chunk * 18;
-#pragma unroll
-    for (int k = 0; k < 18; ++k) qo[k] = res[k];
-  }
-}
-
-
-__global__ __launch_bounds__(128) void k_post(
-    const float* __restrict__ qv_g,
-    const float* __restrict__ op_w, const float* __restrict__ op_b,
-    const float* __restrict__ ln2_g, const float* __restrict__ ln2_b,
-    const float* __restrict__ sa1_w, const float* __restrict__ sa1_b,
-    const float* __restrict__ sa2_w, const float* __restrict__ sa2_b,
+}
+
+
+union MegaU {
+  struct {
+    float xs[kCH][16 * kCHUNK + 4];
+    float hbuf[kCHUNK][132];
+  } pre;
+  float csl[16 * 260];
+};
+
+__global__ __launch_bounds__(128) void k_mega(
+    const float* __restrict__ x,
+    const float* __restrict__ conv_w, const float* __restrict__ conv_b,
+    const float* __restrict__ ln1_g,  const float* __restrict__ ln1_b,
+    const float* __restrict__ ca1_w,  const float* __restrict__ ca1_b,
+    const float* __restrict__ ca2_w,  const float* __restrict__ ca2_b,
+    const float* __restrict__ pp_w,   const float* __restrict__ pp_b,
+    const float* __restrict__ ep_w,   const float* __restrict__ ep_b,
+    const float* __restrict__ op_w,   const float* __restrict__ op_b,
+    const float* __restrict__ ln2_g,  const float* __restrict__ ln2_b,
+    const float* __restrict__ sa1_w,  const float* __restrict__ sa1_b,
+    const float* __restrict__ sa2_w,  const float* __restrict__ sa2_b,
     float* __restrict__ cf, float* __restrict__ sclb)
 {
-  __shared__ float cfs[132];
+  constexpr int NC = 16;
+
+  __shared__ __align__(16) MegaU u;
+  __shared__ __align__(16) float sums[NC][kDM];
+  __shared__ __align__(16) float spart[2][16];
+  __shared__ __align__(16) float wl[kCHUNK];
+  __shared__ float mrow[kCHUNK], irow[kCHUNK];
+  __shared__ __align__(16) float qvs[NC][19];
+  __shared__ __align__(16) float cfs[132];
   __shared__ float part1[32];
   __shared__ float red[4];
 
-  const int chunk = blockIdx.x, tid = threadIdx.x, d = tid;
+  const int tid    = threadIdx.x;
+  const int chunk0 = blockIdx.x * NC;
+  const int b      = chunk0 >> 7;
+  const int tloc   = (chunk0 & 127) * kCHUNK;
+  const int d      = tid;
+  const int lane   = tid & 63;
+  const int wv     = tid >> 6;
+  const int col    = (lane & 15) + 16 * wv;
+  const int qd     = lane >> 4;
+
+  float w12[12];
+  {
+    const float4* cw = (const float4*)(conv_w + d * 12);
+    float4 a0 = cw[0], a1 = cw[1], a2 = cw[2];
+    w12[0]=a0.x; w12[1]=a0.y; w12[2]=a0.z; w12[3]=a0.w;
+    w12[4]=a1.x; w12[5]=a1.y; w12[6]=a1.z; w12[7]=a1.w;
+    w12[8]=a2.x; w12[9]=a2.y; w12[10]=a2.z; w12[11]=a2.w;
+  }
+  float cb = conv_b[d];
+  float g1 = ln1_g[d], b1 = ln1_b[d];
+  float cb1 = ca1_b[col], cw2 = ca2_w[col], cb2 = ca2_b[0];
+
+  bf16x8 bhi[4], blo[4];
+#pragma unroll
+  for (int ks = 0; ks < 4; ++ks)
+#pragma unroll
+    for (int jj = 0; jj < 8; ++jj) {
+      float bvf = ca1_w[(ks * 32 + qd * 8 + jj) * 32 + col];
+      unsigned bb = __float_as_uint(bvf);
+      bhi[ks][jj] = (short)(bb >> 16);
+      float lf = bvf - __uint_as_float(bb & 0xffff0000u);
+      blo[ks][jj] = (short)(__float_as_uint(lf) >> 16);
+    }
+
+#pragma unroll
+  for (int ch = 0; ch < kCH; ++ch) {
+#pragma unroll
+    for (int base = 0; base < 3; ++base) {
+      int pos = base * 128 + tid;
+      if (pos < NC * kCHUNK + 2) {
+        int s = tloc - 1 + pos;
+        float v = 0.f;
+        if (s >= 0 && s < kSEQ) v = x[((size_t)b * kCH + ch) * kSEQ + s];
+        u.pre.xs[ch][pos] = v;
+      }
+    }
+  }
+  __syncthreads();
+
+  for (int c = 0; c < NC; ++c) {
+    float h[kCHUNK];
+#pragma unroll
+    for (int t = 0; t < kCHUNK; ++t) h[t] = cb;
+#pragma unroll
+    for (int ch = 0; ch < kCH; ++ch) {
+      const float4* xp = (const float4*)&u.pre.xs[ch][c * kCHUNK];
+      float4 v0 = xp[0], v1 = xp[1], v2 = xp[2], v3 = xp[3], v4 = xp[4];
+      float xr[18];
+      xr[0]=v0.x; xr[1]=v0.y; xr[2]=v0.z; xr[3]=v0.w;
+      xr[4]=v1.x; xr[5]=v1.y; xr[6]=v1.z; xr[7]=v1.w;
+      xr[8]=v2.x; xr[9]=v2.y; xr[10]=v2.z; xr[11]=v2.w;
+      xr[12]=v3.x; xr[13]=v3.y; xr[14]=v3.z; xr[15]=v3.w;
+      xr[16]=v4.x; xr[17]=v4.y;
+      float c0 = w12[ch*3+0], c1 = w12[ch*3+1], c2 = w12[ch*3+2];
+#pragma unroll
+      for (int t = 0; t < kCHUNK; ++t)
+        h[t] = fmaf(xr[t], c0, fmaf(xr[t+1], c1, fmaf(xr[t+2], c2, h[t])));
+    }
+#pragma unroll
+    for (int t = 0; t < kCHUNK; ++t) u.pre.hbuf[t][d] = h[t];
+    __syncthreads();
+
+    {
+      int row = tid >> 3, k = tid & 7;
+      const float4* rp = (const float4*)&u.pre.hbuf[row][k * 16];
+      float s1 = 0.f, s2 = 0.f;
+#pragma unroll
+      for (int q = 0; q < 4; ++q) {
+        float4 v = rp[q];
+        s1 += v.x + v.y + v.z + v.w;
+        s2 = fmaf(v.x,v.x,s2); s2 = fmaf(v.y,v.y,s2);
+        s2 = fmaf(v.z,v.z,s2); s2 = fmaf(v.w,v.w,s2);
+      }
+#pragma unroll
+      for (int o = 1; o < 8; o <<= 1) {
+        s1 += __shfl_xor(s1, o, 64);
+        s2 += __shfl_xor(s2, o, 64);
+      }
+      if (k == 0) {
+        float m = s1 * (1.f / kDM);
+        mrow[row] = m;
+        irow[row] = rsqrtf(s2 * (1.f / kDM) - m * m + 1e-5f);
+      }
+    }
+    __syncthreads();
+
+#pragma unroll
+    for (int t = 0; t < kCHUNK; ++t) {
+      h[t] = fmaf((h[t] - mrow[t]) * irow[t], g1, b1);
+      unsigned hb = __float_as_uint(h[t]);
+      float lof = h[t] - __uint_as_float(hb & 0xffff0000u);
+      unsigned pk = (hb >> 16) | (__float_as_uint(lof) & 0xffff0000u);
+      ((unsigned*)&u.pre.hbuf[t][0])[d] = pk;
+    }
+    __syncthreads();
+
+    f32x4 acc = {0.f, 0.f, 0.f, 0.f};
+    {
+      const unsigned* hrow = (const unsigned*)&u.pre.hbuf[lane & 15][0];
+#pragma unroll
+      for (int ks = 0; ks < 4; ++ks) {
+        const uint4* ap = (const uint4*)(hrow + ks * 32 + qd * 8);
+        uint4 w0 = ap[0], w1 = ap[1];
+        bf16x8 ahi, alo;
+        ahi[0] = (short)(w0.x & 0xffff); ahi[1] = (short)(w0.y & 0xffff);
+        ahi[2] = (short)(w0.z & 0xffff); ahi[3] = (short)(w0.w & 0xffff);
+        ahi[4] = (short)(w1.x & 0xffff); ahi[5] = (short)(w1.y & 0xffff);
+        ahi[6] = (short)(w1.z & 0xffff); ahi[7] = (short)(w1.w & 0xffff);
+        alo[0] = (short)(w0.x >> 16); alo[1] = (short)(w0.y >> 16);
+        alo[2] = (short)(w0.z >> 16); alo[3] = (short)(w0.w >> 16);
+        alo[4] = (short)(w1.x >> 16); alo[5] = (short)(w1.y >> 16);
+        alo[6] = (short)(w1.z >> 16); alo[7] = (short)(w1.w >> 16);
+        acc = __builtin_amdgcn_mfma_f32_16x16x32_bf16(ahi, bhi[ks], acc, 0, 0, 0);
+        acc = __builtin_amdgcn_mfma_f32_16x16x32_bf16(ahi, blo[ks], acc, 0, 0, 0);
+        acc = __builtin_amdgcn_mfma_f32_16x16x32_bf16(alo, bhi[ks], acc, 0, 0, 0);
+      }
+    }
+
+    {
+      float ev[4];
+#pragma unroll
+      for (int r = 0; r < 4; ++r)
+        ev[r] = fast_tanh(acc[r] + cb1) * cw2;
+#pragma unroll
+      for (int o = 1; o < 16; o <<= 1)
+#pragma unroll
+        for (int r = 0; r < 4; ++r) ev[r] += __shfl_xor(ev[r], o, 64);
+      if ((lane & 15) == 0)
+        *(float4*)&spart[wv][qd * 4] = make_float4(ev[0], ev[1], ev[2], ev[3]);
+    }
+    __syncthreads();
+
+    if (tid < 16) {
+      float scl = spart[0][tid] + spart[1][tid] + cb2;
+      float mx = scl;
+#pragma unroll
+      for (int o = 1; o < 16; o <<= 1) mx = fmaxf(mx, __shfl_xor(mx, o, 64));
+      float e = __expf(scl - mx);
+      float se = e;
+#pragma unroll
+      for (int o = 1; o < 16; o <<= 1) se += __shfl_xor(se, o, 64);
+      wl[tid] = e * (1.f / se);
+    }
+    __syncthreads();
+
+    {
+      const float4* w4 = (const float4*)wl;
+      float4 wa = w4[0], wb = w4[1], wc = w4[2], wd = w4[3];
+      float acc2 = 0.f;
+      acc2 = fmaf(wa.x, h[0],  acc2); acc2 = fmaf(wa.y, h[1],  acc2);
+      acc2 = fmaf(wa.z, h[2],  acc2); acc2 = fmaf(wa.w, h[3],  acc2);
+      acc2 = fmaf(wb.x, h[4],  acc2); acc2 = fmaf(wb.y, h[5],  acc2);
+      acc2 = fmaf(wb.z, h[6],  acc2); acc2 = fmaf(wb.w, h[7],  acc2);
+      acc2 = fmaf(wc.x, h[8],  acc2); acc2 = fmaf(wc.y, h[9],  acc2);
+      acc2 = fmaf(wc.z, h[10], acc2); acc2 = fmaf(wc.w, h[11], acc2);
+      acc2 = fmaf(wd.x, h[12], acc2); acc2 = fmaf(wd.y, h[13], acc2);
+      acc2 = fmaf(wd.z, h[14], acc2); acc2 = fmaf(wd.w, h[15], acc2);
+      sums[c][d] = acc2;
+    }
+  }
+  __syncthreads();
+
+  if (tid < kNP + kNQ) {
+    const bool isep = (tid >= kNP);
+    const int  jj   = tid - kNP;
+    const float* wp = isep ? (ep_w + jj) : (pp_w + tid);
+    const int  ws   = isep ? kNQ : kNP;
+    const int  ws2  = ws * 2, ws3 = ws * 3, ws4 = ws * 4;
+    float bias = isep ? ep_b[jj] : pp_b[tid];
+    float accp[NC];
+#pragma unroll
+    for (int c = 0; c < NC; ++c) accp[c] = bias;
+#pragma unroll 2
+    for (int q4 = 0; q4 < 32; ++q4) {
+      float w0 = wp[0], w1 = wp[ws], w2 = wp[ws2], w3 = wp[ws3];
+      wp += ws4;
+#pragma unroll
+      for (int c = 0; c < NC; ++c) {
+        float4 s = *(const float4*)&sums[c][q4 * 4];
+        accp[c] = fmaf(s.x, w0, fmaf(s.y, w1, fmaf(s.z, w2, fmaf(s.w, w3, accp[c]))));
+      }
+    }
+    const int slot = isep ? jj : (6 + tid);
+#pragma unroll
+    for (int c = 0; c < NC; ++c) {
+      float ha = isep ? (0.5f * fast_tanh(accp[c]) * kPI) : (0.5f * accp[c]);
+      ((float2*)&u.csl[c * 260])[slot] = make_float2(__cosf(ha), __sinf(ha));
+    }
+  }
+  __syncthreads();
+
+  if (tid < 64) {
+    const int c  = tid >> 2;
+    const int l  = tid & 3;
+    const int b0 = (l >> 1) & 1;
+    const int b1 = l & 1;
+    float res[18];
+    circ_from_cs((const float2*)&u.csl[c * 260], l, b0, b1, res);
+    if (l == 0) {
+#pragma unroll
+      for (int k = 0; k < 18; ++k) qvs[c][k] = res[k];
+    }
+  }
+  __syncthreads();
+
   const int j = tid & 31, sub = tid >> 5;
-
-  float qv[18];
-  {
-    const float* qpp = qv_g + (size_t)chunk * 18;
-#pragma unroll
-    for (int k = 0; k < 18; ++k) qv[k] = qpp[k];
-  }
-  float acc = op_b[d];
-#pragma unroll
-  for (int k = 0; k < 18; ++k) acc = fmaf(qv[k], op_w[k * kDM + d], acc);
-
-  float v = acc, v2 = acc * acc;
-#pragma unroll
-  for (int o = 32; o; o >>= 1) { v += __shfl_xor(v, o, 64); v2 += __shfl_xor(v2, o, 64); }
-  if ((tid & 63) == 0) { red[tid >> 6] = v; red[2 + (tid >> 6)] = v2; }
-  __syncthreads();
-  float s1 = red[0] + red[1], s2 = red[2] + red[3];
-  float m = s1 * (1.f / kDM);
-  float var = s2 * (1.f / kDM) - m * m;
-  float xn = fmaf((acc - m) * rsqrtf(var + 1e-5f), ln2_g[d], ln2_b[d]);
-  float cfv = fast_silu(xn);
-  cf[(size_t)chunk * kDM + d] = cfv;
-  cfs[d] = cfv;
-  __syncthreads();
-
-  float acc2 = 0.f;
+  float ow[18];
+#pragma unroll
+  for (int k = 0; k < 18; ++k) ow[k] = op_w[k * kDM + d];
+  float ob = op_b[d], g2 = ln2_g[d], b2 = ln2_b[d];
+  float wreg[32];
   {
     const float* wp2 = sa1_w + (sub * 32) * 32 + j;
+#pragma unroll
+    for (int k = 0; k < 32; ++k) wreg[k] = wp2[k * 32];
+  }
+  float s1bj = sa1_b[j], s2wj = sa2_w[j], s2b = sa2_b[0];
+
+#pragma unroll 1
+  for (int i = 0; i < NC; ++i) {
+    const int chunkg = chunk0 + i;
+
+    float acc = ob;
+#pragma unroll
+    for (int k = 0; k < 18; ++k) acc = fmaf(qvs[i][k], ow[k], acc);
+
+    float v = acc, v2 = acc * acc;
+#pragma unroll
+    for (int o = 32; o; o >>= 1) { v += __shfl_xor(v, o, 64); v2 += __shfl_xor(v2, o, 64); }
+    if ((tid & 63) == 0) { red[tid >> 6] = v; red[2 + (tid >> 6)] = v2; }
+    __syncthreads();
+    float s1 = red[0] + red[1], s2v = red[2] + red[3];
+    float m = s1 * (1.f / kDM);
+    float var = s2v * (1.f / kDM) - m * m;
+    float xn = fmaf((acc - m) * rsqrtf(var + 1e-5f), g2, b2);
+    float cfv = fast_silu(xn);
+    cf[(size_t)chunkg * kDM + d] = cfv;
+    cfs[d] = cfv;
+    __syncthreads();
+
+    float acc2 = 0.f;
 #pragma unroll
     for (int q = 0; q < 8; ++q) {
       float4 hv = *(const float4*)&cfs[sub * 32 + q * 4];
-      acc2 = fmaf(hv.x, wp2[(q*4+0)*32], acc2);
-      acc2 = fmaf(hv.y, wp2[(q*4+1)*32], acc2);
-      acc2 = fmaf(hv.z, wp2[(q*4+2)*32], acc2);
-      acc2 = fmaf(hv.w, wp2[(q*4+3)*32], acc2);
-    }
-  }
-  acc2 += __shfl_xor(acc2, 32, 64);
-  if (sub == 2) part1[j] = acc2;
-  __syncthreads();
-  if (tid < 32) {
-    float hv = fast_tanh(acc2 + part1[j] + sa1_b[j]) * sa2_w[j];
-#pragma unroll
-    for (int o = 16; o; o >>= 1) hv += __shfl_xor(hv, o, 64);
-    if (j == 0) sclb[chunk] = hv + sa2_b[0];
+      acc2 = fmaf(hv.x, wreg[q*4+0], acc2);
+      acc2 = fmaf(hv.y, wreg[q*4+1], acc2);
+      acc2 = fmaf(hv.z, wreg[q*4+2], acc2);
+      acc2 = fmaf(hv.w, wreg[q*4+3], acc2);
+    }
+    acc2 += __shfl_xor(acc2, 32, 64);
+    if (sub == 2) part1[j] = acc2;
+    __syncthreads();
+    if (tid < 32) {
+      float hv = fast_tanh(acc2 + part1[j] + s1bj) * s2wj;
+#pragma unroll
+      for (int o = 16; o; o >>= 1) hv += __shfl_xor(hv, o, 64);
+      if (j == 0) sclb[chunkg] = hv + s2b;
+    }
   }
 }
 
@@ -1017,37 +901,19 @@
   const float* cl2_b  = (const float*)d_in[24];
   float* out = (float*)d_out;
 
-  const size_t nch   = (size_t)kBATCH * kNCH;
-  const size_t fCS   = nch * 256;
-  const size_t need1 = (fCS + nch * 18 + nch) * sizeof(float);
-  const size_t fA    = nch * kDM;
-  const size_t need2 = (fA + nch * 18 + nch) * sizeof(float);
-
-  if (ws_size >= need1) {
-    float* csA   = (float*)d_ws;
-    float* cf    = csA;
-    float* qv_g  = csA + fCS;
-    float* sclb  = qv_g + nch * 18;
-    k_pre8<<<(kBATCH * kNCH) / 8, 128, 0, stream>>>(
+  const size_t nch    = (size_t)kBATCH * kNCH;
+  const size_t fA     = nch * kDM;
+  const size_t need_m = (fA + nch) * sizeof(float);
+
+  if (ws_size >= need_m) {
+    float* cf2  = (float*)d_ws;
+    float* sclb = cf2 + fA;
+    k_mega<<<(kBATCH * kNCH) / 16, 128, 0, stream>>>(
         x, conv_w, conv_b, ln1_g, ln1_b, ca1_w, ca1_b, ca2_w, ca2_b,
-        pp_w, pp_b, ep_w, ep_b, csA, 1);
-    k_circ_cs<<<(kBATCH * kNCH) / 16, 64, 0, stream>>>(csA, qv_g);
-    k_post<<<kBATCH * kNCH, 128, 0, stream>>>(
-        qv_g, op_w, op_b, ln2_g, ln2_b, sa1_w, sa1_b, sa2_w, sa2_b, cf, sclb);
+        pp_w, pp_b, ep_w, ep_b, op_w, op_b, ln2_g, ln2_b,
+        sa1_w, sa1_b, sa2_w, sa2_b, cf2, sclb);
     k_pool_cf<<<kBATCH, 512, 0, stream>>>(
-        cf, sclb, cl1_w, cl1_b, cl2_w, cl2_b, out);
-  } else if (ws_size >= need2) {
-    float* A     = (float*)d_ws;
-    float* qv_g  = A + fA;
-    float* sclb  = qv_g + nch * 18;
-    k_pre8<<<(kBATCH * kNCH) / 8, 128, 0, stream>>>(
-        x, conv_w, conv_b, ln1_g, ln1_b, ca1_w, ca1_b, ca2_w, ca2_b,
-        pp_w, pp_b, ep_w, ep_b, A, 0);
-    k_circ<<<(kBATCH * kNCH) / 16, 64, 0, stream>>>(A, qv_g);
-    k_post<<<kBATCH * kNCH, 128, 0, stream>>>(
-        qv_g, op_w, op_b, ln2_g, ln2_b, sa1_w, sa1_b, sa2_w, sa2_b, A, sclb);
-    k_pool_cf<<<kBATCH, 512, 0, stream>>>(
-        A, sclb, cl1_w, cl1_b, cl2_w, cl2_b, out);
+        cf2, sclb, cl1_w, cl1_b, cl2_w, cl2_b, out);
   } else {
     float* cf   = (float*)d_ws;
     float* sclb = cf + nch * kDM;
```
